# Kernel optimization log

Measured on AMD Instinct MI355X. Metric: run time of the kernel, lower is better.

The kernel has to match this reference:

```python
import jax, jax.numpy as jnp
import numpy as np

B, V, D, E, F, H, HD = 16, 1024, 16, 64, 16, 128, 64
GRAPH_LAYERS, FLOW_ITERS, DUAL_ITERS = 2, 10, 10
STEP, MOM, BIG = 0.01, 0.9, 1e9


def _build_graph():
    # circulant graph: node v's d-th out-neighbor is v + offs[d] (mod V); offsets paired (o, -o)
    offs = np.array([1, -1, 2, -2, 3, -3, 4, -4, 5, -5, 6, -6, 7, -7, 8, -8], dtype=np.int32)
    v = np.arange(V, dtype=np.int32)[:, None]
    d = np.broadcast_to(np.arange(D, dtype=np.int32)[None, :], (V, D))
    adj = ((v + offs[None, :]) % V).astype(np.int32)
    inv_adj = ((v - offs[None, :]) % V).astype(np.int32)
    in_idx = np.stack([inv_adj, d], axis=-1)    # d-th incoming edge of v == out-edge (inv_adj[v,d], slot d)
    rev_idx = np.stack([adj, d], axis=-1)       # out-edge (v,d) is the d-th incoming edge of adj[v,d]
    opp_idx = np.stack([adj, d ^ 1], axis=-1)   # opposite edge (w->v) is slot d^1 at w (paired offsets)
    bt = lambda x: jnp.asarray(np.broadcast_to(x[None], (B,) + x.shape).copy())
    return bt(adj), bt(inv_adj), bt(in_idx), bt(rev_idx), bt(opp_idx)


def setup_inputs() -> dict:
    key = jax.random.key(0)
    ks = jax.random.split(key, 16)
    adj_lst, inv_adj_lst, in_indices, rev_indices, opp_indices = _build_graph()
    rn = lambda k, shape, scale=1.0: jax.random.normal(k, shape, dtype=jnp.float32) * scale
    s = lambda fan: 1.0 / float(np.sqrt(fan))
    return {
        'demands': rn(ks[0], (B, V, 1)),
        'node_features': rn(ks[1], (B, V, F)),
        'edge_lengths': jax.random.uniform(ks[2], (B, V, D), dtype=jnp.float32),
        'norm_edge_lengths': jax.random.uniform(ks[3], (B, V, D), dtype=jnp.float32),
        'node_emb': rn(ks[4], (V, E)),
        'W_enc': rn(ks[5], (E + F, H), s(E + F)), 'b_enc': jnp.zeros((H,), jnp.float32),
        'W_gat': rn(ks[6], (H, H), s(H)), 'b_gat': jnp.zeros((H,), jnp.float32),
        'a_gat': rn(ks[7], (H,), s(H)),
        'W_gru_x': rn(ks[8], (H, 3 * H), s(H)), 'W_gru_h': rn(ks[9], (H, 3 * H), s(H)),
        'b_gru': jnp.zeros((3 * H,), jnp.float32),
        'W_dec1': rn(ks[10], (2 * H, HD), s(2 * H)), 'b_dec1': jnp.zeros((HD,), jnp.float32),
        'W_dec2': rn(ks[11], (HD, 1), s(HD)), 'b_dec2': jnp.zeros((1,), jnp.float32),
        'W_dual1': rn(ks[12], (H, HD), s(H)), 'b_dual1': jnp.zeros((HD,), jnp.float32),
        'W_dual2': rn(ks[13], (HD, 1), s(HD)), 'b_dual2': jnp.zeros((1,), jnp.float32),
        'adj_lst': adj_lst, 'inv_adj_lst': inv_adj_lst,
        'in_indices': in_indices, 'rev_indices': rev_indices, 'opp_indices': opp_indices,
        'num_nodes': jnp.full((B,), V, dtype=jnp.int32),
    }


def _gather_nodes(values, idx, valid):
    # masked_gather with set_zero=True: values (B,V,H), idx (B,V,D) -> (B,V,D,H)
    bb = jnp.arange(values.shape[0])[:, None, None]
    g = values[bb, jnp.clip(idx, 0, values.shape[1] - 1)]
    return g * valid[..., None]


def _gather_edges(x, idx):
    # gather_nd into a (B,V,D,...) tensor; idx (B,V,D,2) = (node, slot), batch implicit
    bb = jnp.arange(x.shape[0])[:, None, None]
    return x[bb, idx[..., 0], idx[..., 1]]


def _sparsemax(z):
    n = z.shape[-1]
    zs = jnp.sort(z, axis=-1)[..., ::-1]
    k = jnp.arange(1, n + 1, dtype=z.dtype)
    zc = jnp.cumsum(zs, axis=-1)
    support = (1.0 + k * zs) > zc
    kz = jnp.sum(support, axis=-1, keepdims=True)
    tau = (jnp.take_along_axis(zc, kz - 1, axis=-1) - 1.0) / kz.astype(z.dtype)
    return jnp.maximum(z - tau, 0.0)


def _forward(demands, node_features, edge_lengths, norm_edge_lengths, node_emb, W_enc, b_enc,
             W_gat, b_gat, a_gat, W_gru_x, W_gru_h, b_gru, W_dec1, b_dec1, W_dec2, b_dec2,
             W_dual1, b_dual1, W_dual2, b_dual2,
             adj_lst, inv_adj_lst, in_indices, rev_indices, opp_indices, num_nodes):
    f32 = jnp.float32
    # embedding lookup with max_norm=1
    nrm = jnp.linalg.norm(node_emb, axis=-1, keepdims=True)
    emb = node_emb / jnp.maximum(nrm, 1.0)
    emb_b = jnp.broadcast_to(emb[None], (demands.shape[0], V, E))
    node_enc = jnp.concatenate([emb_b, node_features], axis=-1) @ W_enc + b_enc   # (B,V,H)
    mask = (adj_lst == num_nodes[:, None, None]).astype(f32)                       # 1 = padded slot
    valid = 1.0 - mask
    initial = _gather_nodes(node_enc, adj_lst, valid)                              # (B,V,D,H)
    h = initial
    for _ in range(GRAPH_LAYERS):
        # DirectionalGAT: per-edge transform, masked attention over slots, directional regather
        t = jnp.tanh(h @ W_gat + b_gat)                                            # (B,V,D,H)
        logits = jnp.einsum('bvdh,h->bvd', t, a_gat) - BIG * mask
        attn = jax.nn.softmax(logits, axis=-1)
        node_msg = jnp.einsum('bvd,bvdh->bvh', attn, t)                            # (B,V,H)
        msg = _gather_nodes(node_msg, adj_lst, valid)
        x = jnp.tanh(msg + initial)
        # GRU cell, shared weights over all edge states
        gx = x @ W_gru_x + b_gru
        gh = h @ W_gru_h
        z = jax.nn.sigmoid(gx[..., :H] + gh[..., :H])
        r = jax.nn.sigmoid(gx[..., H:2 * H] + gh[..., H:2 * H])
        cand = jnp.tanh(gx[..., 2 * H:] + r * gh[..., 2 * H:])
        h = z * h + (1.0 - z) * cand
    # decoder over (encoding, encoding + opposite-edge encoding)
    comb = h + _gather_edges(h, opp_indices)
    dec_in = jnp.concatenate([h, comb], axis=-1)
    nw = (jnp.tanh(dec_in @ W_dec1 + b_dec1) @ W_dec2 + b_dec2)[..., 0]            # (B,V,D)
    # destination attention: normalize over incoming edges, map back to outgoing layout
    inv_mask = (inv_adj_lst == num_nodes[:, None, None]).astype(f32)
    in_w = _gather_edges(nw, in_indices)
    dest_attn = jax.nn.softmax(in_w - BIG * inv_mask, axis=-1)
    nw = _gather_edges(dest_attn, rev_indices)
    pred = nw - BIG * mask
    normalized = _sparsemax(pred) * valid
    # iterative proportional min-cost-flow solver
    def mcf_step(flow, _):
        inflow = jnp.sum(_gather_edges(flow, in_indices), axis=-1, keepdims=True)  # (B,V,1)
        return normalized * jax.nn.relu(inflow - demands), None
    flow, _ = jax.lax.scan(mcf_step, jnp.zeros_like(normalized), None, length=FLOW_ITERS)
    flow_cost = jnp.sum(flow * flow, axis=(1, 2))                                  # square cost fn
    # dual variables + dual flow (projected momentum gradient descent)
    node_states = jnp.sum(h, axis=2)                                               # (B,V,H)
    dual_vars = jax.nn.relu(jnp.tanh(node_states @ W_dual1 + b_dual1) @ W_dual2 + b_dual2)  # (B,V,1)
    dual = mask * dual_vars
    dual_tr = _gather_nodes(dual_vars, adj_lst, valid)[..., 0]
    dual_diff = dual_tr - dual                                                     # (B,V,D)
    def dual_step(carry, _):
        f, vel = carry
        grad = 2.0 * f + dual_diff                                                 # d/df [f^2 + dual_diff*f]
        vel = MOM * vel - STEP * grad
        f = jax.nn.relu(f + vel)
        return (f, vel), None
    (dual_flows, _), _ = jax.lax.scan(dual_step, (jnp.zeros_like(dual_diff), jnp.zeros_like(dual_diff)), None, length=DUAL_ITERS)
    dual_flows = dual_flows * valid
    dual_demand = jnp.sum(dual_vars * demands, axis=(1, 2))
    dual_cost = jnp.sum(dual_flows * dual_flows + dual_diff * dual_flows, axis=(1, 2)) - dual_demand
    return flow_cost - dual_cost                                                   # (B,) primal-dual gap loss


def reference(demands, node_features, edge_lengths, norm_edge_lengths, node_emb, W_enc, b_enc,
              W_gat, b_gat, a_gat, W_gru_x, W_gru_h, b_gru, W_dec1, b_dec1, W_dec2, b_dec2,
              W_dual1, b_dual1, W_dual2, b_dual2,
              adj_lst, inv_adj_lst, in_indices, rev_indices, opp_indices, num_nodes):
    return _forward(demands, node_features, edge_lengths, norm_edge_lengths, node_emb, W_enc, b_enc,
                    W_gat, b_gat, a_gat, W_gru_x, W_gru_h, b_gru, W_dec1, b_dec1, W_dec2, b_dec2,
                    W_dual1, b_dual1, W_dual2, b_dual2,
                    adj_lst, inv_adj_lst, in_indices, rev_indices, opp_indices, num_nodes)
```

## Files before the change

### kernel.cpp

```cpp
#include <hip/hip_runtime.h>
#include <hip/hip_bf16.h>

#define B 16
#define V 1024
#define D 16
#define E 64
#define F 16
#define H 128
#define HD 64
#define BV (B*V)
#define BVD (B*V*D)

#define OFF_HNB      0
#define OFF_NORM     (OFF_HNB + BV*H/2)
#define OFF_DV       (OFF_NORM + BVD)
#define OFF_WT       (OFF_DV + BV)
#define OFF_WTG      (OFF_WT + 65536)
#define OFF_WPQ      (OFF_WTG + 8192)
#define OFF_WU1T     (OFF_WPQ + 8192)
#define OFF_WENCT    (OFF_WU1T + 4096)

typedef __attribute__((ext_vector_type(8))) short bf16x8;
typedef __attribute__((ext_vector_type(4))) float f32x4;

__device__ __forceinline__ short f2bf(float f){
  __hip_bfloat16 b = __float2bfloat16(f);
  return *reinterpret_cast<short*>(&b);
}
__device__ __forceinline__ float bf2f(short s){
  __hip_bfloat16 b; *reinterpret_cast<short*>(&b) = s;
  return __bfloat162float(b);
}
__device__ __forceinline__ float frcp(float x){ return __builtin_amdgcn_rcpf(x); }
__device__ __forceinline__ float fsig(float x){ return frcp(1.f + __expf(-x)); }
__device__ __forceinline__ float ftanh(float x){
  float e = __expf(-2.f*fabsf(x));
  float r = (1.f - e)*frcp(1.f + e);
  return copysignf(r, x);
}

__global__ __launch_bounds__(256) void k_pre(const float* __restrict__ Wx, const float* __restrict__ Wh,
    const float* __restrict__ Wg, const float* __restrict__ W1, const float* __restrict__ Wu1,
    const float* __restrict__ Wenc,
    short* __restrict__ Wt, short* __restrict__ Wgt, short* __restrict__ Wpq,
    short* __restrict__ Wu1t, short* __restrict__ Wenct, float* __restrict__ outz){
  int bid = blockIdx.x, tid = threadIdx.x;
  if (bid == 0 && tid < 16) outz[tid] = 0.f;
  if (bid < 512){
    int n = bid, k = tid;
    int g = n >> 7, j = n & 127;
    float v;
    if (g == 0)      v = (k < 128) ? Wx[k*384 + j]       : Wh[(k-128)*384 + j];
    else if (g == 1) v = (k < 128) ? Wx[k*384 + 128 + j] : Wh[(k-128)*384 + 128 + j];
    else if (g == 2) v = (k < 128) ? Wx[k*384 + 256 + j] : 0.f;
    else             v = (k < 128) ? 0.f                 : Wh[(k-128)*384 + 256 + j];
    Wt[n*256 + k] = f2bf(v);
    return;
  }
  if (bid < 576){
    int idx = (bid-512)*256 + tid;
    int n = idx >> 7, k = idx & 127;
    Wgt[n*128 + k] = f2bf(Wg[k*128 + n]);
    return;
  }
  if (bid < 608){
    int idx = (bid-576)*256 + tid;
    int n = idx >> 7, k = idx & 127;
    float wb = W1[(k+128)*HD + n];
    float wa = W1[k*HD + n];
    Wpq[n*128 + k]      = f2bf(wa + wb);
    Wpq[(64+n)*128 + k] = f2bf(wb);
    return;
  }
  if (bid < 640){
    int idx = (bid-608)*256 + tid;
    int n = idx >> 7, k = idx & 127;
    Wu1t[n*128 + k] = f2bf(Wu1[k*HD + n]);
    return;
  }
  {
    int nn = (bid-640)*2 + (tid >> 7);
    int kk = tid & 127;
    if (kk < 96) Wenct[nn*96 + kk] = f2bf(kk < 80 ? Wenc[kk*128 + nn] : 0.f);
  }
}

__global__ __launch_bounds__(512,2) void k_mega(const float* __restrict__ emb, const float* __restrict__ nf,
    const short* __restrict__ Wenct, const float* __restrict__ benc, const int* __restrict__ adj,
    const short* __restrict__ Wgt, const float* __restrict__ bg, const float* __restrict__ ag,
    const short* __restrict__ Wt, const float* __restrict__ bgru, short* __restrict__ hout){
  __shared__ short NE[96][136];
  __shared__ short Tt[128][104];
  __shared__ short H1[80][136];
  __shared__ short X[80][136];
  __shared__ short A2[80][104];
  __shared__ float Lp[8][96];
  __shared__ float Ls[96];
  __shared__ float nrmv[96];
  short (*As)[104] = reinterpret_cast<short(*)[104]>(&H1[0][0]);

  int tid = threadIdx.x;
  int blk = blockIdx.x;
  int b = blk >> 4;
  int n0 = (blk & 15) << 6;
  int w = tid >> 6, lane = tid & 63;
  int l15 = lane & 15, quad = lane >> 4;

  int li96[16];
  if (tid < 80){
    int wg = (b<<10) + ((n0 - 8 + tid) & 1023);
    const int4* a4 = reinterpret_cast<const int4*>(&adj[(long)wg*16]);
    #pragma unroll
    for (int d4=0; d4<4; d4++){
      int4 i4 = a4[d4];
      li96[d4*4+0] = (i4.x - n0 + 16) & 1023;
      li96[d4*4+1] = (i4.y - n0 + 16) & 1023;
      li96[d4*4+2] = (i4.z - n0 + 16) & 1023;
      li96[d4*4+3] = (i4.w - n0 + 16) & 1023;
    }
  }

  if (tid < 384){
    int r = tid >> 2, q = tid & 3;
    int v = (n0 - 16 + r) & 1023;
    const float4* e4 = reinterpret_cast<const float4*>(&emb[v*E]);
    float ss = 0.f;
    #pragma unroll
    for (int qq=0;qq<4;qq++){ float4 x = e4[q*4+qq]; ss += x.x*x.x + x.y*x.y + x.z*x.z + x.w*x.w; }
    ss += __shfl_xor(ss, 1);
    ss += __shfl_xor(ss, 2);
    if (q == 0) nrmv[r] = frcp(fmaxf(sqrtf(ss), 1.f));
  }
  __syncthreads();
  for (int e=tid; e<96*16; e+=512){
    int r = e >> 4, q = e & 15;
    int v = (n0 - 16 + r) & 1023;
    float4 x = reinterpret_cast<const float4*>(&emb[v*E])[q];
    float iv = nrmv[r];
    short4 s; s.x=f2bf(x.x*iv); s.y=f2bf(x.y*iv); s.z=f2bf(x.z*iv); s.w=f2bf(x.w*iv);
    *reinterpret_cast<short4*>(&As[r][q*4]) = s;
  }
  for (int e=tid; e<96*4; e+=512){
    int r = e >> 2, q = e & 3;
    int m = (b<<10) + ((n0 - 16 + r) & 1023);
    float4 x = reinterpret_cast<const float4*>(&nf[(long)m*F])[q];
    short4 s; s.x=f2bf(x.x); s.y=f2bf(x.y); s.z=f2bf(x.z); s.w=f2bf(x.w);
    *reinterpret_cast<short4*>(&As[r][64 + q*4]) = s;
    short4 z; z.x=0; z.y=0; z.z=0; z.w=0;
    *reinterpret_cast<short4*>(&As[r][80 + q*4]) = z;
  }
  __syncthreads();
  {
    f32x4 acc[6];
    #pragma unroll
    for (int mt=0;mt<6;mt++) acc[mt] = (f32x4){0.f,0.f,0.f,0.f};
    #pragma unroll
    for (int kc=0;kc<3;kc++){
      int k0 = kc*32;
      bf16x8 bfr = *reinterpret_cast<const bf16x8*>(&Wenct[(16*w + l15)*96 + k0 + quad*8]);
      #pragma unroll
      for (int mt=0;mt<6;mt++){
        bf16x8 a = *reinterpret_cast<const bf16x8*>(&As[16*mt + l15][k0 + quad*8]);
        acc[mt] = __builtin_amdgcn_mfma_f32_16x16x32_bf16(a, bfr, acc[mt], 0,0,0);
      }
    }
    int c = 16*w + l15;
    float bb = benc[c];
    #pragma unroll
    for (int mt=0;mt<6;mt++)
      #pragma unroll
      for (int reg=0;reg<4;reg++)
        NE[16*mt + quad*4 + reg][c] = f2bf(acc[mt][reg] + bb);
  }
  __syncthreads();
  {
    f32x4 acc[6];
    #pragma unroll
    for (int mt=0;mt<6;mt++) acc[mt] = (f32x4){0.f,0.f,0.f,0.f};
    #pragma unroll
    for (int kc=0;kc<4;kc++){
      int k0 = kc*32;
      bf16x8 bfr = *reinterpret_cast<const bf16x8*>(&Wgt[(16*w + l15)*128 + k0 + quad*8]);
      #pragma unroll
      for (int mt=0;mt<6;mt++){
        bf16x8 a = *reinterpret_cast<const bf16x8*>(&NE[16*mt + l15][k0 + quad*8]);
        acc[mt] = __builtin_amdgcn_mfma_f32_16x16x32_bf16(a, bfr, acc[mt], 0,0,0);
      }
    }
    int c = 16*w + l15;
    float bgc = bg[c], agc = ag[c];
    float lp[6][4];
    #pragma unroll
    for (int mt=0;mt<6;mt++){
      short4 tv;
      #pragma unroll
      for (int reg=0;reg<4;reg++){
        float t = ftanh(acc[mt][reg] + bgc);
        reinterpret_cast<short*>(&tv)[reg] = f2bf(t);
        lp[mt][reg] = t * agc;
      }
      *reinterpret_cast<short4*>(&Tt[c][16*mt + quad*4]) = tv;
    }
    #pragma unroll
    for (int mt=0;mt<6;mt++)
      #pragma unroll
      for (int reg=0;reg<4;reg++){
        lp[mt][reg] += __shfl_xor(lp[mt][reg], 1);
        lp[mt][reg] += __shfl_xor(lp[mt][reg], 2);
        lp[mt][reg] += __shfl_xor(lp[mt][reg], 4);
        lp[mt][reg] += __shfl_xor(lp[mt][reg], 8);
      }
    if (l15 == 0){
      #pragma unroll
      for (int mt=0;mt<6;mt++)
        #pragma unroll
        for (int reg=0;reg<4;reg++)
          Lp[w][16*mt + quad*4 + reg] = lp[mt][reg];
    }
  }
  __syncthreads();
  if (tid < 96){
    float s = 0.f;
    #pragma unroll
    for (int i=0;i<8;i++) s += Lp[i][tid];
    Ls[tid] = s;
  }
  {
    bf16x8 z8;
    #pragma unroll
    for (int q=0;q<8;q++) z8[q] = 0;
    for (int idx=tid; idx<960; idx+=512){
      int r = idx/12, c8 = idx%12;
      *reinterpret_cast<bf16x8*>(&A2[r][c8*8]) = z8;
    }
  }
  __syncthreads();
  if (tid < 80){
    float at[16];
    float m = -1e30f;
    #pragma unroll
    for (int d=0; d<16; d++) m = fmaxf(m, Ls[li96[d]]);
    float s = 0.f;
    #pragma unroll
    for (int d=0; d<16; d++){ at[d] = __expf(Ls[li96[d]] - m); s += at[d]; }
    float inv = frcp(s);
    #pragma unroll
    for (int d=0; d<16; d++) A2[tid][li96[d]] = f2bf(at[d]*inv);
  }
  __syncthreads();
  {
    f32x4 acc[5];
    #pragma unroll
    for (int mt=0;mt<5;mt++) acc[mt] = (f32x4){0.f,0.f,0.f,0.f};
    #pragma unroll
    for (int kc=0;kc<3;kc++){
      int k0 = kc*32;
      bf16x8 bfr = *reinterpret_cast<const bf16x8*>(&Tt[16*w + l15][k0 + quad*8]);
      #pragma unroll
      for (int mt=0;mt<5;mt++){
        bf16x8 a = *reinterpret_cast<const bf16x8*>(&A2[16*mt + l15][k0 + quad*8]);
        acc[mt] = __builtin_amdgcn_mfma_f32_16x16x32_bf16(a, bfr, acc[mt], 0,0,0);
      }
    }
    int c = 16*w + l15;
    #pragma unroll
    for (int mt=0;mt<5;mt++)
      #pragma unroll
      for (int reg=0;reg<4;reg++){
        int rl = 16*mt + quad*4 + reg;
        X[rl][c] = f2bf(ftanh(acc[mt][reg] + bf2f(NE[rl + 8][c])));
      }
  }
  __syncthreads();
  {
    f32x4 acc[5][4];
    #pragma unroll
    for (int mt=0;mt<5;mt++)
      #pragma unroll
      for (int g=0;g<4;g++) acc[mt][g] = (f32x4){0.f,0.f,0.f,0.f};
    for (int k8=0;k8<8;k8++){
      int k0 = k8*32;
      int gg = (k8 < 4) ? 2 : 3;
      int ncol = 16*w + l15;
      int koff = k0 + quad*8;
      bf16x8 bz = *reinterpret_cast<const bf16x8*>(&Wt[(ncol      )*256 + koff]);
      bf16x8 br = *reinterpret_cast<const bf16x8*>(&Wt[(ncol + 128)*256 + koff]);
      bf16x8 bc = *reinterpret_cast<const bf16x8*>(&Wt[(ncol + gg*128)*256 + koff]);
      #pragma unroll
      for (int mt=0;mt<5;mt++){
        bf16x8 a;
        if (k8 < 4) a = *reinterpret_cast<const bf16x8*>(&X[16*mt + l15][k0 + quad*8]);
        else        a = *reinterpret_cast<const bf16x8*>(&NE[16*mt + l15 + 8][k0 - 128 + quad*8]);
        acc[mt][0]  = __builtin_amdgcn_mfma_f32_16x16x32_bf16(a, bz, acc[mt][0], 0,0,0);
        acc[mt][1]  = __builtin_amdgcn_mfma_f32_16x16x32_bf16(a, br, acc[mt][1], 0,0,0);
        acc[mt][gg] = __builtin_amdgcn_mfma_f32_16x16x32_bf16(a, bc, acc[mt][gg], 0,0,0);
      }
    }
    int j = 16*w + l15;
    float bjz = bgru[j], bjr = bgru[128 + j], bjc = bgru[256 + j];
    #pragma unroll
    for (int mt=0;mt<5;mt++){
      #pragma unroll
      for (int reg=0;reg<4;reg++){
        int rl = 16*mt + quad*4 + reg;
        float z = fsig(acc[mt][0][reg] + bjz);
        float r = fsig(acc[mt][1][reg] + bjr);
        float cand = ftanh(acc[mt][2][reg] + bjc + r*acc[mt][3][reg]);
        float ho = bf2f(NE[rl + 8][j]);
        H1[rl][j] = f2bf(z*ho + (1.f - z)*cand);
      }
    }
  }
  __syncthreads();
  {
    f32x4 acc[5];
    #pragma unroll
    for (int mt=0;mt<5;mt++) acc[mt] = (f32x4){0.f,0.f,0.f,0.f};
    #pragma unroll
    for (int kc=0;kc<4;kc++){
      int k0 = kc*32;
      bf16x8 bfr = *reinterpret_cast<const bf16x8*>(&Wgt[(16*w + l15)*128 + k0 + quad*8]);
      #pragma unroll
      for (int mt=0;mt<5;mt++){
        bf16x8 a = *reinterpret_cast<const bf16x8*>(&H1[16*mt + l15][k0 + quad*8]);
        acc[mt] = __builtin_amdgcn_mfma_f32_16x16x32_bf16(a, bfr, acc[mt], 0,0,0);
      }
    }
    int c = 16*w + l15;
    float bgc = bg[c], agc = ag[c];
    float lp[5][4];
    #pragma unroll
    for (int mt=0;mt<5;mt++){
      short4 tv;
      #pragma unroll
      for (int reg=0;reg<4;reg++){
        float t = ftanh(acc[mt][reg] + bgc);
        reinterpret_cast<short*>(&tv)[reg] = f2bf(t);
        lp[mt][reg] = t * agc;
      }
      *reinterpret_cast<short4*>(&Tt[c][16*mt + quad*4]) = tv;
    }
    #pragma unroll
    for (int mt=0;mt<5;mt++)
      #pragma unroll
      for (int reg=0;reg<4;reg++){
        lp[mt][reg] += __shfl_xor(lp[mt][reg], 1);
        lp[mt][reg] += __shfl_xor(lp[mt][reg], 2);
        lp[mt][reg] += __shfl_xor(lp[mt][reg], 4);
        lp[mt][reg] += __shfl_xor(lp[mt][reg], 8);
      }
    if (l15 == 0){
      #pragma unroll
      for (int mt=0;mt<5;mt++)
        #pragma unroll
        for (int reg=0;reg<4;reg++)
          Lp[w][16*mt + quad*4 + reg] = lp[mt][reg];
    }
  }
  __syncthreads();
  if (tid < 80){
    float s = 0.f;
    #pragma unroll
    for (int i=0;i<8;i++) s += Lp[i][tid];
    Ls[tid] = s;
  }
  {
    bf16x8 z8;
    #pragma unroll
    for (int q=0;q<8;q++) z8[q] = 0;
    for (int idx=tid; idx<768; idx+=512){
      int r = idx/12, c8 = idx%12;
      *reinterpret_cast<bf16x8*>(&A2[r][c8*8]) = z8;
    }
  }
  __syncthreads();
  if (tid >= 8 && tid < 72){
    int r5 = tid - 8;
    float at[16];
    float m = -1e30f;
    #pragma unroll
    for (int d=0; d<16; d++) m = fmaxf(m, Ls[li96[d] - 8]);
    float s = 0.f;
    #pragma unroll
    for (int d=0; d<16; d++){ at[d] = __expf(Ls[li96[d] - 8] - m); s += at[d]; }
    float inv = frcp(s);
    #pragma unroll
    for (int d=0; d<16; d++) A2[r5][li96[d] - 8] = f2bf(at[d]*inv);
  }
  __syncthreads();
  {
    f32x4 acc[4];
    #pragma unroll
    for (int mt=0;mt<4;mt++) acc[mt] = (f32x4){0.f,0.f,0.f,0.f};
    #pragma unroll
    for (int kc=0;kc<3;kc++){
      int k0 = kc*32;
      bf16x8 bfr = *reinterpret_cast<const bf16x8*>(&Tt[16*w + l15][k0 + quad*8]);
      #pragma unroll
      for (int mt=0;mt<4;mt++){
        bf16x8 a = *reinterpret_cast<const bf16x8*>(&A2[16*mt + l15][k0 + quad*8]);
        acc[mt] = __builtin_amdgcn_mfma_f32_16x16x32_bf16(a, bfr, acc[mt], 0,0,0);
      }
    }
    int c = 16*w + l15;
    #pragma unroll
    for (int mt=0;mt<4;mt++)
      #pragma unroll
      for (int reg=0;reg<4;reg++){
        int rl = 16*mt + quad*4 + reg;
        X[rl][c] = f2bf(ftanh(acc[mt][reg] + bf2f(NE[rl + 16][c])));
      }
  }
  __syncthreads();
  {
    f32x4 acc[4][4];
    #pragma unroll
    for (int mt=0;mt<4;mt++)
      #pragma unroll
      for (int g=0;g<4;g++) acc[mt][g] = (f32x4){0.f,0.f,0.f,0.f};
    for (int k8=0;k8<8;k8++){
      int k0 = k8*32;
      int gg = (k8 < 4) ? 2 : 3;
      int ncol = 16*w + l15;
      int koff = k0 + quad*8;
      bf16x8 bz = *reinterpret_cast<const bf16x8*>(&Wt[(ncol      )*256 + koff]);
      bf16x8 br = *reinterpret_cast<const bf16x8*>(&Wt[(ncol + 128)*256 + koff]);
      bf16x8 bc = *reinterpret_cast<const bf16x8*>(&Wt[(ncol + gg*128)*256 + koff]);
      #pragma unroll
      for (int mt=0;mt<4;mt++){
        bf16x8 a;
        if (k8 < 4) a = *reinterpret_cast<const bf16x8*>(&X[16*mt + l15][k0 + quad*8]);
        else        a = *reinterpret_cast<const bf16x8*>(&H1[16*mt + l15 + 8][k0 - 128 + quad*8]);
        acc[mt][0]  = __builtin_amdgcn_mfma_f32_16x16x32_bf16(a, bz, acc[mt][0], 0,0,0);
        acc[mt][1]  = __builtin_amdgcn_mfma_f32_16x16x32_bf16(a, br, acc[mt][1], 0,0,0);
        acc[mt][gg] = __builtin_amdgcn_mfma_f32_16x16x32_bf16(a, bc, acc[mt][gg], 0,0,0);
      }
    }
    __syncthreads();
    int j = 16*w + l15;
    float bjz = bgru[j], bjr = bgru[128 + j], bjc = bgru[256 + j];
    #pragma unroll
    for (int mt=0;mt<4;mt++){
      #pragma unroll
      for (int reg=0;reg<4;reg++){
        int rl = 16*mt + quad*4 + reg;
        float z = fsig(acc[mt][0][reg] + bjz);
        float r = fsig(acc[mt][1][reg] + bjr);
        float cand = ftanh(acc[mt][2][reg] + bjc + r*acc[mt][3][reg]);
        float ho = bf2f(H1[rl + 8][j]);
        X[rl][j] = f2bf(z*ho + (1.f - z)*cand);
      }
    }
  }
  __syncthreads();
  for (int idx=tid; idx<64*16; idx+=512){
    int r = idx >> 4, c8 = idx & 15;
    *reinterpret_cast<bf16x8*>(&hout[(long)((b<<10) + n0 + r)*128 + c8*8]) =
        *reinterpret_cast<const bf16x8*>(&X[r][c8*8]);
  }
}

__global__ __launch_bounds__(1024,4) void k_decdas(const short* __restrict__ hn, const int* __restrict__ adj,
    const int* __restrict__ invadj, const short* __restrict__ Wpq, const float* __restrict__ b1,
    const float* __restrict__ W2, const float* __restrict__ b2_,
    const short* __restrict__ Wu1t, const float* __restrict__ bu1, const float* __restrict__ Wu2,
    const float* __restrict__ bu2_, float* __restrict__ norm_, float* __restrict__ dv){
  __shared__ short Hs[112][136];
  __shared__ short PQb[112][132];
  __shared__ short NSs[64][136];
  __shared__ int adjL[64][16];
  __shared__ float dvp[64][4];
  __shared__ float b1s[64], w2s[64], bu1s[64], wu2s[64];
  int tid = threadIdx.x;
  int blk = blockIdx.x;
  int b = blk >> 4;
  int n0 = (blk & 15) << 6;
  if (tid < 64){ b1s[tid] = b1[tid]; w2s[tid] = W2[tid]; bu1s[tid] = bu1[tid]; wu2s[tid] = Wu2[tid]; }
  for (int idx=tid; idx<112*16; idx+=1024){
    int r = idx >> 4, c8 = idx & 15;
    int g = (b << 10) + ((n0 - 24 + r) & 1023);
    *reinterpret_cast<bf16x8*>(&Hs[r][c8*8]) =
        *reinterpret_cast<const bf16x8*>(&hn[(long)g*128 + c8*8]);
  }
  {
    int r = tid >> 4, d = tid & 15;
    int a = adj[((b<<10) + n0 + r)*16 + d];
    adjL[r][d] = (a - n0 + 24) & 1023;
  }
  __syncthreads();
  int w = tid >> 6, lane = tid & 63;
  int l15 = lane & 15, quad = lane >> 4;
  int cw = w & 7, hw = w >> 3;
  {
    f32x4 acc[4];
    #pragma unroll
    for (int t=0;t<4;t++) acc[t] = (f32x4){0.f,0.f,0.f,0.f};
    #pragma unroll
    for (int kc=0;kc<4;kc++){
      int k0 = kc*32;
      bf16x8 bfr = *reinterpret_cast<const bf16x8*>(&Wpq[(16*cw + l15)*128 + k0 + quad*8]);
      #pragma unroll
      for (int t=0;t<4;t++){
        int mt = 4*hw + t;
        if (mt < 7){
          bf16x8 a = *reinterpret_cast<const bf16x8*>(&Hs[16*mt + l15][k0 + quad*8]);
          acc[t] = __builtin_amdgcn_mfma_f32_16x16x32_bf16(a, bfr, acc[t], 0,0,0);
        }
      }
    }
    int c = 16*cw + l15;
    #pragma unroll
    for (int t=0;t<4;t++){
      int mt = 4*hw + t;
      if (mt < 7){
        #pragma unroll
        for (int reg=0;reg<4;reg++)
          PQb[16*mt + quad*4 + reg][c] = f2bf(acc[t][reg]);
      }
    }
  }
  {
    int r = tid >> 4, c8 = tid & 15;
    float acc8[8] = {0,0,0,0,0,0,0,0};
    #pragma unroll 4
    for (int d=0; d<16; d++){
      bf16x8 hv = *reinterpret_cast<const bf16x8*>(&Hs[adjL[r][d]][c8*8]);
      #pragma unroll
      for (int q=0;q<8;q++) acc8[q] += bf2f(hv[q]);
    }
    bf16x8 sv;
    #pragma unroll
    for (int q=0;q<8;q++) sv[q] = f2bf(acc8[q]);
    *reinterpret_cast<bf16x8*>(&NSs[r][c8*8]) = sv;
  }
  __syncthreads();
  if (w < 8){
    int c4 = w & 3, h2 = w >> 2;
    f32x4 acc[2];
    #pragma unroll
    for (int t=0;t<2;t++) acc[t] = (f32x4){0.f,0.f,0.f,0.f};
    #pragma unroll
    for (int kc=0;kc<4;kc++){
      int k0 = kc*32;
      bf16x8 bfr = *reinterpret_cast<const bf16x8*>(&Wu1t[(16*c4 + l15)*128 + k0 + quad*8]);
      #pragma unroll
      for (int t=0;t<2;t++){
        bf16x8 a = *reinterpret_cast<const bf16x8*>(&NSs[16*(2*h2+t) + l15][k0 + quad*8]);
        acc[t] = __builtin_amdgcn_mfma_f32_16x16x32_bf16(a, bfr, acc[t], 0,0,0);
      }
    }
    int n = 16*c4 + l15;
    float bn = bu1s[n], wn = wu2s[n];
    #pragma unroll
    for (int t=0;t<2;t++){
      #pragma unroll
      for (int reg=0;reg<4;reg++){
        float p = ftanh(acc[t][reg] + bn) * wn;
        p += __shfl_xor(p, 1);
        p += __shfl_xor(p, 2);
        p += __shfl_xor(p, 4);
        p += __shfl_xor(p, 8);
        if (l15 == 0) dvp[16*(2*h2+t) + quad*4 + reg][c4] = p;
      }
    }
  }
  __syncthreads();
  float* nws = reinterpret_cast<float*>(&Hs[0][0]);
  float b2v = b2_[0];
  for (int e = tid; e < 96*16; e += 1024){
    int rr = e >> 4, d = e & 15;
    int wnode = (n0 + rr - 16) & 1023;
    int wg = (b<<10) + wnode;
    int a = adj[wg*16 + d];
    int al = (a - n0 + 24) & 1023;
    int wl = rr + 8;
    float p = 0.f;
    #pragma unroll 8
    for (int c=0;c<64;c++)
      p += ftanh(bf2f(PQb[al][c]) + bf2f(PQb[wl][64 + c]) + b1s[c]) * w2s[c];
    nws[rr*17 + d] = p + b2v;
  }
  __syncthreads();
  if (tid < 64){
    float val = dvp[tid][0]+dvp[tid][1]+dvp[tid][2]+dvp[tid][3];
    dv[(b<<10) + n0 + tid] = fmaxf(val + bu2_[0], 0.f);
  }
  float* datt = reinterpret_cast<float*>(&PQb[0][0]);
  if (tid < 80){
    int wnode = (n0 + tid - 8) & 1023;
    int wg = (b<<10) + wnode;
    float vals[16];
    float m = -1e30f;
    #pragma unroll
    for (int d=0; d<16; d++){
      int iv = invadj[wg*16 + d];
      int il = (iv - n0 + 16) & 1023;
      vals[d] = nws[il*17 + d];
      m = fmaxf(m, vals[d]);
    }
    float s = 0.f;
    #pragma unroll
    for (int d=0; d<16; d++){ vals[d] = __expf(vals[d]-m); s += vals[d]; }
    float inv = frcp(s);
    #pragma unroll
    for (int d=0; d<16; d++) datt[tid*17 + d] = vals[d]*inv;
  }
  __syncthreads();
  if (tid < 64){
    int vg = (b<<10) + n0 + tid;
    float z[16], s[16];
    #pragma unroll
    for (int d=0; d<16; d++){
      int al = adjL[tid][d] - 16;
      z[d] = datt[al*17 + d];
      s[d] = z[d];
    }
    #pragma unroll
    for (int k2 = 2; k2 <= 16; k2 <<= 1){
      #pragma unroll
      for (int jj = k2 >> 1; jj > 0; jj >>= 1){
        #pragma unroll
        for (int i = 0; i < 16; i++){
          int l = i ^ jj;
          if (l > i){
            bool up = ((i & k2) == 0);
            float a = s[i], bb = s[l];
            bool sw = up ? (a > bb) : (a < bb);
            if (sw){ s[i]=bb; s[l]=a; }
          }
        }
      }
    }
    float cs = 0.f, zcs = 0.f; int kz = 1;
    #pragma unroll
    for (int j=0;j<16;j++){
      float zj = s[15-j];
      cs += zj;
      if (1.f + (float)(j+1)*zj > cs){ kz = j+1; zcs = cs; }
    }
    float tau = (zcs - 1.f)/(float)kz;
    #pragma unroll
    for (int d=0; d<16; d++) norm_[(long)vg*16 + d] = fmaxf(z[d]-tau, 0.f);
  }
}

__global__ __launch_bounds__(256) void k_flowfin(const float* __restrict__ norm_,
    const float* __restrict__ dem, const int* __restrict__ invadj, const float* __restrict__ dv,
    float* __restrict__ out){
  __shared__ float nrmS[224*17];
  __shared__ float sbuf[2][224];
  __shared__ float red[4];
  int tid = threadIdx.x;
  int blk = blockIdx.x;
  int b = blk >> 4;
  int t0 = (blk & 15) << 6;
  for (int e=tid; e<224*4; e+=256){
    int r = e >> 2, q4 = e & 3;
    int v = (t0 - 80 + r) & 1023;
    float4 x = reinterpret_cast<const float4*>(&norm_[(long)((b<<10) + v)*16])[q4];
    nrmS[r*17 + q4*4+0] = x.x; nrmS[r*17 + q4*4+1] = x.y;
    nrmS[r*17 + q4*4+2] = x.z; nrmS[r*17 + q4*4+3] = x.w;
  }
  bool act = tid < 224;
  int r = tid;
  float dm = 0.f; int gv = 0;
  int ivl[16];
  if (act){
    int v = (t0 - 80 + r) & 1023;
    gv = (b<<10) + v;
    dm = dem[gv];
    #pragma unroll
    for (int d4=0; d4<4; d4++){
      int4 i4 = reinterpret_cast<const int4*>(&invadj[(long)gv*16])[d4];
      int t;
      t = (i4.x - t0 + 80) & 1023; ivl[d4*4+0] = t < 224 ? t : 223;
      t = (i4.y - t0 + 80) & 1023; ivl[d4*4+1] = t < 224 ? t : 223;
      t = (i4.z - t0 + 80) & 1023; ivl[d4*4+2] = t < 224 ? t : 223;
      t = (i4.w - t0 + 80) & 1023; ivl[d4*4+3] = t < 224 ? t : 223;
    }
    sbuf[0][r] = 0.f;
  }
  __syncthreads();
  float nrg[16];
  if (act){
    #pragma unroll
    for (int d=0; d<16; d++) nrg[d] = nrmS[ivl[d]*17 + d];
  }
  int p = 0;
  float s = 0.f;
  for (int it=0; it<10; it++){
    if (act){
      float inflow = 0.f;
      #pragma unroll
      for (int d=0; d<16; d++) inflow += nrg[d]*sbuf[p][ivl[d]];
      s = fmaxf(inflow - dm, 0.f);
      sbuf[1-p][r] = s;
    }
    p ^= 1;
    __syncthreads();
  }
  float partF = 0.f, partD = 0.f, partDD = 0.f;
  if (act && r >= 80 && r < 144){
    float nr2 = 0.f;
    #pragma unroll
    for (int d=0; d<16; d++){ float nv = nrmS[r*17 + d]; nr2 += nv*nv; }
    partF = nr2 * s * s;
    float dvv = dv[gv];
    float f = 0.f, vel = 0.f;
    #pragma unroll
    for (int it=0; it<10; it++){
      float g = 2.f*f + dvv;
      vel = 0.9f*vel - 0.01f*g;
      f = fmaxf(f + vel, 0.f);
    }
    partD = f*f + dvv*f;
    partDD = dvv * dm;
  }
  float val = partF - 16.f*partD + partDD;
  #pragma unroll
  for (int off=32; off>0; off>>=1) val += __shfl_down(val, off);
  if ((tid & 63) == 0) red[tid>>6] = val;
  __syncthreads();
  if (tid == 0) atomicAdd(&out[b], red[0]+red[1]+red[2]+red[3]);
}

extern "C" void kernel_launch(void* const* d_in, const int* in_sizes, int n_in,
                              void* d_out, int out_size, void* d_ws, size_t ws_size,
                              hipStream_t stream){
  (void)in_sizes; (void)n_in; (void)out_size; (void)ws_size;
  const float* demands = (const float*)d_in[0];
  const float* nf      = (const float*)d_in[1];
  const float* emb     = (const float*)d_in[4];
  const float* Wenc    = (const float*)d_in[5];
  const float* benc    = (const float*)d_in[6];
  const float* Wgat    = (const float*)d_in[7];
  const float* bgat    = (const float*)d_in[8];
  const float* agat    = (const float*)d_in[9];
  const float* Wgx     = (const float*)d_in[10];
  const float* Wgh     = (const float*)d_in[11];
  const float* bgru    = (const float*)d_in[12];
  const float* Wd1     = (const float*)d_in[13];
  const float* bd1     = (const float*)d_in[14];
  const float* Wd2     = (const float*)d_in[15];
  const float* bd2     = (const float*)d_in[16];
  const float* Wu1     = (const float*)d_in[17];
  const float* bu1     = (const float*)d_in[18];
  const float* Wu2     = (const float*)d_in[19];
  const float* bu2     = (const float*)d_in[20];
  const int* adj       = (const int*)d_in[21];
  const int* invadj    = (const int*)d_in[22];

  float* ws    = (float*)d_ws;
  short* hnB   = (short*)(ws + OFF_HNB);
  float* nrm   = ws + OFF_NORM;
  float* dv    = ws + OFF_DV;
  short* wt    = (short*)(ws + OFF_WT);
  short* wtg   = (short*)(ws + OFF_WTG);
  short* wpq   = (short*)(ws + OFF_WPQ);
  short* wu1t  = (short*)(ws + OFF_WU1T);
  short* wenct = (short*)(ws + OFF_WENCT);

  k_pre<<<704, 256, 0, stream>>>(Wgx, Wgh, Wgat, Wd1, Wu1, Wenc, wt, wtg, wpq, wu1t, wenct,
                                 (float*)d_out);
  k_mega<<<BV/64, 512, 0, stream>>>(emb, nf, wenct, benc, adj, wtg, bgat, agat, wt, bgru, hnB);
  k_decdas<<<BV/64, 1024, 0, stream>>>(hnB, adj, invadj, wpq, bd1, Wd2, bd2,
                                       wu1t, bu1, Wu2, bu2, nrm, dv);
  k_flowfin<<<B*16, 256, 0, stream>>>(nrm, demands, invadj, dv, (float*)d_out);
}
```

Baseline: 176.6 us.

## Fuse GNN, decoder and flow kernels into one cooperative kernel with grid syncs

Merges the three per-tile kernels (GNN encoder/GAT/GRU, decoder plus dual attention, flow iterations) into a single cooperative launch. Stages are separated by grid-wide syncs and share a union of shared-memory layouts. The decoder stage now runs with 512 threads instead of 1024, with its loops adjusted to match. This removes kernel launch gaps and tail effects but adds grid-barrier cost, and the merged stages may limit occupancy because of register and shared-memory pressure.

```diff
diff --git a/kernel.cpp b/kernel.cpp
--- a/kernel.cpp
+++ b/kernel.cpp
@@ -1,5 +1,8 @@
 #include <hip/hip_runtime.h>
+#include <hip/hip_cooperative_groups.h>
 #include <hip/hip_bf16.h>
+
+namespace cg = cooperative_groups;
 
 #define B 16
 #define V 1024
@@ -85,19 +88,42 @@
   }
 }
 
-__global__ __launch_bounds__(512,2) void k_mega(const float* __restrict__ emb, const float* __restrict__ nf,
+__global__ __launch_bounds__(512,2) void k_fused(
+    const float* __restrict__ emb, const float* __restrict__ nf,
     const short* __restrict__ Wenct, const float* __restrict__ benc, const int* __restrict__ adj,
     const short* __restrict__ Wgt, const float* __restrict__ bg, const float* __restrict__ ag,
-    const short* __restrict__ Wt, const float* __restrict__ bgru, short* __restrict__ hout){
-  __shared__ short NE[96][136];
-  __shared__ short Tt[128][104];
-  __shared__ short H1[80][136];
-  __shared__ short X[80][136];
-  __shared__ short A2[80][104];
-  __shared__ float Lp[8][96];
-  __shared__ float Ls[96];
-  __shared__ float nrmv[96];
-  short (*As)[104] = reinterpret_cast<short(*)[104]>(&H1[0][0]);
+    const short* __restrict__ Wt, const float* __restrict__ bgru, short* __restrict__ hout,
+    const int* __restrict__ invadj, const short* __restrict__ Wpq, const float* __restrict__ b1,
+    const float* __restrict__ W2, const float* __restrict__ b2_,
+    const short* __restrict__ Wu1t, const float* __restrict__ bu1, const float* __restrict__ Wu2,
+    const float* __restrict__ bu2_,
+    float* __restrict__ norm_, float* __restrict__ dv,
+    const float* __restrict__ dem, float* __restrict__ out){
+  __shared__ union {
+    struct {
+      short NE[96][136];
+      short Tt[128][104];
+      short H1[80][136];
+      short X[80][136];
+      short A2[80][104];
+      float Lp[8][96];
+      float Ls[96];
+      float nrmv[96];
+    } a;
+    struct {
+      short Hs[112][136];
+      short PQb[112][132];
+      short NSs[64][136];
+      int adjL[64][16];
+      float dvp[64][4];
+      float b1s[64], w2s[64], bu1s[64], wu2s[64];
+    } b;
+    struct {
+      float nrmS[224*17];
+      float sbuf[2][224];
+      float red[8];
+    } c;
+  } U;
 
   int tid = threadIdx.x;
   int blk = blockIdx.x;
@@ -106,622 +132,613 @@
   int w = tid >> 6, lane = tid & 63;
   int l15 = lane & 15, quad = lane >> 4;
 
-  int li96[16];
-  if (tid < 80){
-    int wg = (b<<10) + ((n0 - 8 + tid) & 1023);
-    const int4* a4 = reinterpret_cast<const int4*>(&adj[(long)wg*16]);
+  {
+    auto& NE = U.a.NE; auto& Tt = U.a.Tt; auto& H1 = U.a.H1; auto& X = U.a.X;
+    auto& A2 = U.a.A2; auto& Lp = U.a.Lp; auto& Ls = U.a.Ls; auto& nrmv = U.a.nrmv;
+    short (*As)[104] = reinterpret_cast<short(*)[104]>(&H1[0][0]);
+
+    int li96[16];
+    if (tid < 80){
+      int wg = (b<<10) + ((n0 - 8 + tid) & 1023);
+      const int4* a4 = reinterpret_cast<const int4*>(&adj[(long)wg*16]);
+      #pragma unroll
+      for (int d4=0; d4<4; d4++){
+        int4 i4 = a4[d4];
+        li96[d4*4+0] = (i4.x - n0 + 16) & 1023;
+        li96[d4*4+1] = (i4.y - n0 + 16) & 1023;
+        li96[d4*4+2] = (i4.z - n0 + 16) & 1023;
+        li96[d4*4+3] = (i4.w - n0 + 16) & 1023;
+      }
+    }
+
+    if (tid < 384){
+      int r = tid >> 2, q = tid & 3;
+      int v = (n0 - 16 + r) & 1023;
+      const float4* e4 = reinterpret_cast<const float4*>(&emb[v*E]);
+      float ss = 0.f;
+      #pragma unroll
+      for (int qq=0;qq<4;qq++){ float4 x = e4[q*4+qq]; ss += x.x*x.x + x.y*x.y + x.z*x.z + x.w*x.w; }
+      ss += __shfl_xor(ss, 1);
+      ss += __shfl_xor(ss, 2);
+      if (q == 0) nrmv[r] = frcp(fmaxf(sqrtf(ss), 1.f));
+    }
+    __syncthreads();
+    for (int e=tid; e<96*16; e+=512){
+      int r = e >> 4, q = e & 15;
+      int v = (n0 - 16 + r) & 1023;
+      float4 x = reinterpret_cast<const float4*>(&emb[v*E])[q];
+      float iv = nrmv[r];
+      short4 s; s.x=f2bf(x.x*iv); s.y=f2bf(x.y*iv); s.z=f2bf(x.z*iv); s.w=f2bf(x.w*iv);
+      *reinterpret_cast<short4*>(&As[r][q*4]) = s;
+    }
+    for (int e=tid; e<96*4; e+=512){
+      int r = e >> 2, q = e & 3;
+      int m = (b<<10) + ((n0 - 16 + r) & 1023);
+      float4 x = reinterpret_cast<const float4*>(&nf[(long)m*F])[q];
+      short4 s; s.x=f2bf(x.x); s.y=f2bf(x.y); s.z=f2bf(x.z); s.w=f2bf(x.w);
+      *reinterpret_cast<short4*>(&As[r][64 + q*4]) = s;
+      short4 z; z.x=0; z.y=0; z.z=0; z.w=0;
+      *reinterpret_cast<short4*>(&As[r][80 + q*4]) = z;
+    }
+    __syncthreads();
+    {
+      f32x4 acc[6];
+      #pragma unroll
+      for (int mt=0;mt<6;mt++) acc[mt] = (f32x4){0.f,0.f,0.f,0.f};
+      #pragma unroll
+      for (int kc=0;kc<3;kc++){
+        int k0 = kc*32;
+        bf16x8 bfr = *reinterpret_cast<const bf16x8*>(&Wenct[(16*w + l15)*96 + k0 + quad*8]);
+        #pragma unroll
+        for (int mt=0;mt<6;mt++){
+          bf16x8 a = *reinterpret_cast<const bf16x8*>(&As[16*mt + l15][k0 + quad*8]);
+          acc[mt] = __builtin_amdgcn_mfma_f32_16x16x32_bf16(a, bfr, acc[mt], 0,0,0);
+        }
+      }
+      int c = 16*w + l15;
+      float bb = benc[c];
+      #pragma unroll
+      for (int mt=0;mt<6;mt++)
+        #pragma unroll
+        for (int reg=0;reg<4;reg++)
+          NE[16*mt + quad*4 + reg][c] = f2bf(acc[mt][reg] + bb);
+    }
+    __syncthreads();
+    {
+      f32x4 acc[6];
+      #pragma unroll
+      for (int mt=0;mt<6;mt++) acc[mt] = (f32x4){0.f,0.f,0.f,0.f};
+      #pragma unroll
+      for (int kc=0;kc<4;kc++){
+        int k0 = kc*32;
+        bf16x8 bfr = *reinterpret_cast<const bf16x8*>(&Wgt[(16*w + l15)*128 + k0 + quad*8]);
+        #pragma unroll
+        for (int mt=0;mt<6;mt++){
+          bf16x8 a = *reinterpret_cast<const bf16x8*>(&NE[16*mt + l15][k0 + quad*8]);
+          acc[mt] = __builtin_amdgcn_mfma_f32_16x16x32_bf16(a, bfr, acc[mt], 0,0,0);
+        }
+      }
+      int c = 16*w + l15;
+      float bgc = bg[c], agc = ag[c];
+      float lp[6][4];
+      #pragma unroll
+      for (int mt=0;mt<6;mt++){
+        short4 tv;
+        #pragma unroll
+        for (int reg=0;reg<4;reg++){
+          float t = ftanh(acc[mt][reg] + bgc);
+          reinterpret_cast<short*>(&tv)[reg] = f2bf(t);
+          lp[mt][reg] = t * agc;
+        }
+        *reinterpret_cast<short4*>(&Tt[c][16*mt + quad*4]) = tv;
+      }
+      #pragma unroll
+      for (int mt=0;mt<6;mt++)
+        #pragma unroll
+        for (int reg=0;reg<4;reg++){
+          lp[mt][reg] += __shfl_xor(lp[mt][reg], 1);
+          lp[mt][reg] += __shfl_xor(lp[mt][reg], 2);
+          lp[mt][reg] += __shfl_xor(lp[mt][reg], 4);
+          lp[mt][reg] += __shfl_xor(lp[mt][reg], 8);
+        }
+      if (l15 == 0){
+        #pragma unroll
+        for (int mt=0;mt<6;mt++)
+          #pragma unroll
+          for (int reg=0;reg<4;reg++)
+            Lp[w][16*mt + quad*4 + reg] = lp[mt][reg];
+      }
+    }
+    __syncthreads();
+    if (tid < 96){
+      float s = 0.f;
+      #pragma unroll
+      for (int i=0;i<8;i++) s += Lp[i][tid];
+      Ls[tid] = s;
+    }
+    {
+      bf16x8 z8;
+      #pragma unroll
+      for (int q=0;q<8;q++) z8[q] = 0;
+      for (int idx=tid; idx<960; idx+=512){
+        int r = idx/12, c8 = idx%12;
+        *reinterpret_cast<bf16x8*>(&A2[r][c8*8]) = z8;
+      }
+    }
+    __syncthreads();
+    if (tid < 80){
+      float at[16];
+      float m = -1e30f;
+      #pragma unroll
+      for (int d=0; d<16; d++) m = fmaxf(m, Ls[li96[d]]);
+      float s = 0.f;
+      #pragma unroll
+      for (int d=0; d<16; d++){ at[d] = __expf(Ls[li96[d]] - m); s += at[d]; }
+      float inv = frcp(s);
+      #pragma unroll
+      for (int d=0; d<16; d++) A2[tid][li96[d]] = f2bf(at[d]*inv);
+    }
+    __syncthreads();
+    {
+      f32x4 acc[5];
+      #pragma unroll
+      for (int mt=0;mt<5;mt++) acc[mt] = (f32x4){0.f,0.f,0.f,0.f};
+      #pragma unroll
+      for (int kc=0;kc<3;kc++){
+        int k0 = kc*32;
+        bf16x8 bfr = *reinterpret_cast<const bf16x8*>(&Tt[16*w + l15][k0 + quad*8]);
+        #pragma unroll
+        for (int mt=0;mt<5;mt++){
+          bf16x8 a = *reinterpret_cast<const bf16x8*>(&A2[16*mt + l15][k0 + quad*8]);
+          acc[mt] = __builtin_amdgcn_mfma_f32_16x16x32_bf16(a, bfr, acc[mt], 0,0,0);
+        }
+      }
+      int c = 16*w + l15;
+      #pragma unroll
+      for (int mt=0;mt<5;mt++)
+        #pragma unroll
+        for (int reg=0;reg<4;reg++){
+          int rl = 16*mt + quad*4 + reg;
+          X[rl][c] = f2bf(ftanh(acc[mt][reg] + bf2f(NE[rl + 8][c])));
+        }
+    }
+    __syncthreads();
+    {
+      f32x4 acc[5][4];
+      #pragma unroll
+      for (int mt=0;mt<5;mt++)
+        #pragma unroll
+        for (int g=0;g<4;g++) acc[mt][g] = (f32x4){0.f,0.f,0.f,0.f};
+      for (int k8=0;k8<8;k8++){
+        int k0 = k8*32;
+        int gg = (k8 < 4) ? 2 : 3;
+        int ncol = 16*w + l15;
+        int koff = k0 + quad*8;
+        bf16x8 bz = *reinterpret_cast<const bf16x8*>(&Wt[(ncol      )*256 + koff]);
+        bf16x8 br = *reinterpret_cast<const bf16x8*>(&Wt[(ncol + 128)*256 + koff]);
+        bf16x8 bc = *reinterpret_cast<const bf16x8*>(&Wt[(ncol + gg*128)*256 + koff]);
+        #pragma unroll
+        for (int mt=0;mt<5;mt++){
+          bf16x8 a;
+          if (k8 < 4) a = *reinterpret_cast<const bf16x8*>(&X[16*mt + l15][k0 + quad*8]);
+          else        a = *reinterpret_cast<const bf16x8*>(&NE[16*mt + l15 + 8][k0 - 128 + quad*8]);
+          acc[mt][0]  = __builtin_amdgcn_mfma_f32_16x16x32_bf16(a, bz, acc[mt][0], 0,0,0);
+          acc[mt][1]  = __builtin_amdgcn_mfma_f32_16x16x32_bf16(a, br, acc[mt][1], 0,0,0);
+          acc[mt][gg] = __builtin_amdgcn_mfma_f32_16x16x32_bf16(a, bc, acc[mt][gg], 0,0,0);
+        }
+      }
+      int j = 16*w + l15;
+      float bjz = bgru[j], bjr = bgru[128 + j], bjc = bgru[256 + j];
+      #pragma unroll
+      for (int mt=0;mt<5;mt++){
+        #pragma unroll
+        for (int reg=0;reg<4;reg++){
+          int rl = 16*mt + quad*4 + reg;
+          float z = fsig(acc[mt][0][reg] + bjz);
+          float r = fsig(acc[mt][1][reg] + bjr);
+          float cand = ftanh(acc[mt][2][reg] + bjc + r*acc[mt][3][reg]);
+          float ho = bf2f(NE[rl + 8][j]);
+          H1[rl][j] = f2bf(z*ho + (1.f - z)*cand);
+        }
+      }
+    }
+    __syncthreads();
+    {
+      f32x4 acc[5];
+      #pragma unroll
+      for (int mt=0;mt<5;mt++) acc[mt] = (f32x4){0.f,0.f,0.f,0.f};
+      #pragma unroll
+      for (int kc=0;kc<4;kc++){
+        int k0 = kc*32;
+        bf16x8 bfr = *reinterpret_cast<const bf16x8*>(&Wgt[(16*w + l15)*128 + k0 + quad*8]);
+        #pragma unroll
+        for (int mt=0;mt<5;mt++){
+          bf16x8 a = *reinterpret_cast<const bf16x8*>(&H1[16*mt + l15][k0 + quad*8]);
+          acc[mt] = __builtin_amdgcn_mfma_f32_16x16x32_bf16(a, bfr, acc[mt], 0,0,0);
+        }
+      }
+      int c = 16*w + l15;
+      float bgc = bg[c], agc = ag[c];
+      float lp[5][4];
+      #pragma unroll
+      for (int mt=0;mt<5;mt++){
+        short4 tv;
+        #pragma unroll
+        for (int reg=0;reg<4;reg++){
+          float t = ftanh(acc[mt][reg] + bgc);
+          reinterpret_cast<short*>(&tv)[reg] = f2bf(t);
+          lp[mt][reg] = t * agc;
+        }
+        *reinterpret_cast<short4*>(&Tt[c][16*mt + quad*4]) = tv;
+      }
+      #pragma unroll
+      for (int mt=0;mt<5;mt++)
+        #pragma unroll
+        for (int reg=0;reg<4;reg++){
+          lp[mt][reg] += __shfl_xor(lp[mt][reg], 1);
+          lp[mt][reg] += __shfl_xor(lp[mt][reg], 2);
+          lp[mt][reg] += __shfl_xor(lp[mt][reg], 4);
+          lp[mt][reg] += __shfl_xor(lp[mt][reg], 8);
+        }
+      if (l15 == 0){
+        #pragma unroll
+        for (int mt=0;mt<5;mt++)
+          #pragma unroll
+          for (int reg=0;reg<4;reg++)
+            Lp[w][16*mt + quad*4 + reg] = lp[mt][reg];
+      }
+    }
+    __syncthreads();
+    if (tid < 80){
+      float s = 0.f;
+      #pragma unroll
+      for (int i=0;i<8;i++) s += Lp[i][tid];
+      Ls[tid] = s;
+    }
+    {
+      bf16x8 z8;
+      #pragma unroll
+      for (int q=0;q<8;q++) z8[q] = 0;
+      for (int idx=tid; idx<768; idx+=512){
+        int r = idx/12, c8 = idx%12;
+        *reinterpret_cast<bf16x8*>(&A2[r][c8*8]) = z8;
+      }
+    }
+    __syncthreads();
+    if (tid >= 8 && tid < 72){
+      int r5 = tid - 8;
+      float at[16];
+      float m = -1e30f;
+      #pragma unroll
+      for (int d=0; d<16; d++) m = fmaxf(m, Ls[li96[d] - 8]);
+      float s = 0.f;
+      #pragma unroll
+      for (int d=0; d<16; d++){ at[d] = __expf(Ls[li96[d] - 8] - m); s += at[d]; }
+      float inv = frcp(s);
+      #pragma unroll
+      for (int d=0; d<16; d++) A2[r5][li96[d] - 8] = f2bf(at[d]*inv);
+    }
+    __syncthreads();
+    {
+      f32x4 acc[4];
+      #pragma unroll
+      for (int mt=0;mt<4;mt++) acc[mt] = (f32x4){0.f,0.f,0.f,0.f};
+      #pragma unroll
+      for (int kc=0;kc<3;kc++){
+        int k0 = kc*32;
+        bf16x8 bfr = *reinterpret_cast<const bf16x8*>(&Tt[16*w + l15][k0 + quad*8]);
+        #pragma unroll
+        for (int mt=0;mt<4;mt++){
+          bf16x8 a = *reinterpret_cast<const bf16x8*>(&A2[16*mt + l15][k0 + quad*8]);
+          acc[mt] = __builtin_amdgcn_mfma_f32_16x16x32_bf16(a, bfr, acc[mt], 0,0,0);
+        }
+      }
+      int c = 16*w + l15;
+      #pragma unroll
+      for (int mt=0;mt<4;mt++)
+        #pragma unroll
+        for (int reg=0;reg<4;reg++){
+          int rl = 16*mt + quad*4 + reg;
+          X[rl][c] = f2bf(ftanh(acc[mt][reg] + bf2f(NE[rl + 16][c])));
+        }
+    }
+    __syncthreads();
+    {
+      f32x4 acc[4][4];
+      #pragma unroll
+      for (int mt=0;mt<4;mt++)
+        #pragma unroll
+        for (int g=0;g<4;g++) acc[mt][g] = (f32x4){0.f,0.f,0.f,0.f};
+      for (int k8=0;k8<8;k8++){
+        int k0 = k8*32;
+        int gg = (k8 < 4) ? 2 : 3;
+        int ncol = 16*w + l15;
+        int koff = k0 + quad*8;
+        bf16x8 bz = *reinterpret_cast<const bf16x8*>(&Wt[(ncol      )*256 + koff]);
+        bf16x8 br = *reinterpret_cast<const bf16x8*>(&Wt[(ncol + 128)*256 + koff]);
+        bf16x8 bc = *reinterpret_cast<const bf16x8*>(&Wt[(ncol + gg*128)*256 + koff]);
+        #pragma unroll
+        for (int mt=0;mt<4;mt++){
+          bf16x8 a;
+          if (k8 < 4) a = *reinterpret_cast<const bf16x8*>(&X[16*mt + l15][k0 + quad*8]);
+          else        a = *reinterpret_cast<const bf16x8*>(&H1[16*mt + l15 + 8][k0 - 128 + quad*8]);
+          acc[mt][0]  = __builtin_amdgcn_mfma_f32_16x16x32_bf16(a, bz, acc[mt][0], 0,0,0);
+          acc[mt][1]  = __builtin_amdgcn_mfma_f32_16x16x32_bf16(a, br, acc[mt][1], 0,0,0);
+          acc[mt][gg] = __builtin_amdgcn_mfma_f32_16x16x32_bf16(a, bc, acc[mt][gg], 0,0,0);
+        }
+      }
+      __syncthreads();
+      int j = 16*w + l15;
+      float bjz = bgru[j], bjr = bgru[128 + j], bjc = bgru[256 + j];
+      #pragma unroll
+      for (int mt=0;mt<4;mt++){
+        #pragma unroll
+        for (int reg=0;reg<4;reg++){
+          int rl = 16*mt + quad*4 + reg;
+          float z = fsig(acc[mt][0][reg] + bjz);
+          float r = fsig(acc[mt][1][reg] + bjr);
+          float cand = ftanh(acc[mt][2][reg] + bjc + r*acc[mt][3][reg]);
+          float ho = bf2f(H1[rl + 8][j]);
+          X[rl][j] = f2bf(z*ho + (1.f - z)*cand);
+        }
+      }
+    }
+    __syncthreads();
+    for (int idx=tid; idx<64*16; idx+=512){
+      int r = idx >> 4, c8 = idx & 15;
+      *reinterpret_cast<bf16x8*>(&hout[(long)((b<<10) + n0 + r)*128 + c8*8]) =
+          *reinterpret_cast<const bf16x8*>(&X[r][c8*8]);
+    }
+  }
+
+  __threadfence();
+  cg::this_grid().sync();
+
+  {
+    auto& Hs = U.b.Hs; auto& PQb = U.b.PQb; auto& NSs = U.b.NSs;
+    auto& adjL = U.b.adjL; auto& dvp = U.b.dvp;
+    float* b1s = U.b.b1s; float* w2s = U.b.w2s; float* bu1s = U.b.bu1s; float* wu2s = U.b.wu2s;
+
+    if (tid < 64){ b1s[tid] = b1[tid]; w2s[tid] = W2[tid]; bu1s[tid] = bu1[tid]; wu2s[tid] = Wu2[tid]; }
+    for (int idx=tid; idx<112*16; idx+=512){
+      int r = idx >> 4, c8 = idx & 15;
+      int g = (b << 10) + ((n0 - 24 + r) & 1023);
+      *reinterpret_cast<bf16x8*>(&Hs[r][c8*8]) =
+          *reinterpret_cast<const bf16x8*>(&hout[(long)g*128 + c8*8]);
+    }
+    for (int idx=tid; idx<1024; idx+=512){
+      int r = idx >> 4, d = idx & 15;
+      int a = adj[((b<<10) + n0 + r)*16 + d];
+      adjL[r][d] = (a - n0 + 24) & 1023;
+    }
+    __syncthreads();
+    {
+      f32x4 acc[7];
+      #pragma unroll
+      for (int mt=0;mt<7;mt++) acc[mt] = (f32x4){0.f,0.f,0.f,0.f};
+      #pragma unroll
+      for (int kc=0;kc<4;kc++){
+        int k0 = kc*32;
+        bf16x8 bfr = *reinterpret_cast<const bf16x8*>(&Wpq[(16*w + l15)*128 + k0 + quad*8]);
+        #pragma unroll
+        for (int mt=0;mt<7;mt++){
+          bf16x8 a = *reinterpret_cast<const bf16x8*>(&Hs[16*mt + l15][k0 + quad*8]);
+          acc[mt] = __builtin_amdgcn_mfma_f32_16x16x32_bf16(a, bfr, acc[mt], 0,0,0);
+        }
+      }
+      int c = 16*w + l15;
+      #pragma unroll
+      for (int mt=0;mt<7;mt++)
+        #pragma unroll
+        for (int reg=0;reg<4;reg++)
+          PQb[16*mt + quad*4 + reg][c] = f2bf(acc[mt][reg]);
+    }
+    for (int idx=tid; idx<64*16; idx+=512){
+      int r = idx >> 4, c8 = idx & 15;
+      float acc8[8] = {0,0,0,0,0,0,0,0};
+      #pragma unroll 4
+      for (int d=0; d<16; d++){
+        bf16x8 hv = *reinterpret_cast<const bf16x8*>(&Hs[adjL[r][d]][c8*8]);
+        #pragma unroll
+        for (int q=0;q<8;q++) acc8[q] += bf2f(hv[q]);
+      }
+      bf16x8 sv;
+      #pragma unroll
+      for (int q=0;q<8;q++) sv[q] = f2bf(acc8[q]);
+      *reinterpret_cast<bf16x8*>(&NSs[r][c8*8]) = sv;
+    }
+    __syncthreads();
+    if (w < 4){
+      f32x4 acc[4];
+      #pragma unroll
+      for (int mt=0;mt<4;mt++) acc[mt] = (f32x4){0.f,0.f,0.f,0.f};
+      #pragma unroll
+      for (int kc=0;kc<4;kc++){
+        int k0 = kc*32;
+        bf16x8 bfr = *reinterpret_cast<const bf16x8*>(&Wu1t[(16*w + l15)*128 + k0 + quad*8]);
+        #pragma unroll
+        for (int mt=0;mt<4;mt++){
+          bf16x8 a = *reinterpret_cast<const bf16x8*>(&NSs[16*mt + l15][k0 + quad*8]);
+          acc[mt] = __builtin_amdgcn_mfma_f32_16x16x32_bf16(a, bfr, acc[mt], 0,0,0);
+        }
+      }
+      int n = 16*w + l15;
+      float bn = bu1s[n], wn = wu2s[n];
+      #pragma unroll
+      for (int mt=0;mt<4;mt++){
+        #pragma unroll
+        for (int reg=0;reg<4;reg++){
+          float p = ftanh(acc[mt][reg] + bn) * wn;
+          p += __shfl_xor(p, 1);
+          p += __shfl_xor(p, 2);
+          p += __shfl_xor(p, 4);
+          p += __shfl_xor(p, 8);
+          if (l15 == 0) dvp[16*mt + quad*4 + reg][w] = p;
+        }
+      }
+    }
+    __syncthreads();
+    float* nws = reinterpret_cast<float*>(&Hs[0][0]);
+    float b2v = b2_[0];
+    for (int e = tid; e < 96*16; e += 512){
+      int rr = e >> 4, d = e & 15;
+      int wnode = (n0 + rr - 16) & 1023;
+      int wg = (b<<10) + wnode;
+      int a = adj[wg*16 + d];
+      int al = (a - n0 + 24) & 1023;
+      int wl = rr + 8;
+      float p = 0.f;
+      #pragma unroll 8
+      for (int c=0;c<64;c++)
+        p += ftanh(bf2f(PQb[al][c]) + bf2f(PQb[wl][64 + c]) + b1s[c]) * w2s[c];
+      nws[rr*17 + d] = p + b2v;
+    }
+    __syncthreads();
+    if (tid < 64){
+      float val = dvp[tid][0]+dvp[tid][1]+dvp[tid][2]+dvp[tid][3];
+      dv[(b<<10) + n0 + tid] = fmaxf(val + bu2_[0], 0.f);
+    }
+    float* datt = reinterpret_cast<float*>(&PQb[0][0]);
+    if (tid < 80){
+      int wnode = (n0 + tid - 8) & 1023;
+      int wg = (b<<10) + wnode;
+      float vals[16];
+      float m = -1e30f;
+      #pragma unroll
+      for (int d=0; d<16; d++){
+        int iv = invadj[wg*16 + d];
+        int il = (iv - n0 + 16) & 1023;
+        vals[d] = nws[il*17 + d];
+        m = fmaxf(m, vals[d]);
+      }
+      float s = 0.f;
+      #pragma unroll
+      for (int d=0; d<16; d++){ vals[d] = __expf(vals[d]-m); s += vals[d]; }
+      float inv = frcp(s);
+      #pragma unroll
+      for (int d=0; d<16; d++) datt[tid*17 + d] = vals[d]*inv;
+    }
+    __syncthreads();
+    if (tid < 64){
+      int vg = (b<<10) + n0 + tid;
+      float z[16], s[16];
+      #pragma unroll
+      for (int d=0; d<16; d++){
+        int al = adjL[tid][d] - 16;
+        z[d] = datt[al*17 + d];
+        s[d] = z[d];
+      }
+      #pragma unroll
+      for (int k2 = 2; k2 <= 16; k2 <<= 1){
+        #pragma unroll
+        for (int jj = k2 >> 1; jj > 0; jj >>= 1){
+          #pragma unroll
+          for (int i = 0; i < 16; i++){
+            int l = i ^ jj;
+            if (l > i){
+              bool up = ((i & k2) == 0);
+              float a = s[i], bb = s[l];
+              bool sw = up ? (a > bb) : (a < bb);
+              if (sw){ s[i]=bb; s[l]=a; }
+            }
+          }
+        }
+      }
+      float cs = 0.f, zcs = 0.f; int kz = 1;
+      #pragma unroll
+      for (int j=0;j<16;j++){
+        float zj = s[15-j];
+        cs += zj;
+        if (1.f + (float)(j+1)*zj > cs){ kz = j+1; zcs = cs; }
+      }
+      float tau = (zcs - 1.f)/(float)kz;
+      #pragma unroll
+      for (int d=0; d<16; d++) norm_[(long)vg*16 + d] = fmaxf(z[d]-tau, 0.f);
+    }
+  }
+
+  __threadfence();
+  cg::this_grid().sync();
+
+  {
+    float* nrmS = U.c.nrmS;
+    auto& sbuf = U.c.sbuf;
+    float* red = U.c.red;
+    int t0 = n0;
+    for (int e=tid; e<224*4; e+=512){
+      int r = e >> 2, q4 = e & 3;
+      int v = (t0 - 80 + r) & 1023;
+      float4 x = reinterpret_cast<const float4*>(&norm_[(long)((b<<10) + v)*16])[q4];
+      nrmS[r*17 + q4*4+0] = x.x; nrmS[r*17 + q4*4+1] = x.y;
+      nrmS[r*17 + q4*4+2] = x.z; nrmS[r*17 + q4*4+3] = x.w;
+    }
+    bool act = tid < 224;
+    int r = tid;
+    float dm = 0.f; int gv = 0;
+    int ivl[16];
+    if (act){
+      int v = (t0 - 80 + r) & 1023;
+      gv = (b<<10) + v;
+      dm = dem[gv];
+      #pragma unroll
+      for (int d4=0; d4<4; d4++){
+        int4 i4 = reinterpret_cast<const int4*>(&invadj[(long)gv*16])[d4];
+        int t;
+        t = (i4.x - t0 + 80) & 1023; ivl[d4*4+0] = t < 224 ? t : 223;
+        t = (i4.y - t0 + 80) & 1023; ivl[d4*4+1] = t < 224 ? t : 223;
+        t = (i4.z - t0 + 80) & 1023; ivl[d4*4+2] = t < 224 ? t : 223;
+        t = (i4.w - t0 + 80) & 1023; ivl[d4*4+3] = t < 224 ? t : 223;
+      }
+      sbuf[0][r] = 0.f;
+    }
+    __syncthreads();
+    float nrg[16];
+    if (act){
+      #pragma unroll
+      for (int d=0; d<16; d++) nrg[d] = nrmS[ivl[d]*17 + d];
+    }
+    int p = 0;
+    float s = 0.f;
+    for (int it=0; it<10; it++){
+      if (act){
+        float inflow = 0.f;
+        #pragma unroll
+        for (int d=0; d<16; d++) inflow += nrg[d]*sbuf[p][ivl[d]];
+        s = fmaxf(inflow - dm, 0.f);
+        sbuf[1-p][r] = s;
+      }
+      p ^= 1;
+      __syncthreads();
+    }
+    float partF = 0.f, partD = 0.f, partDD = 0.f;
+    if (act && r >= 80 && r < 144){
+      float nr2 = 0.f;
+      #pragma unroll
+      for (int d=0; d<16; d++){ float nv = nrmS[r*17 + d]; nr2 += nv*nv; }
+      partF = nr2 * s * s;
+      float dvv = dv[gv];
+      float f = 0.f, vel = 0.f;
+      #pragma unroll
+      for (int it=0; it<10; it++){
+        float g = 2.f*f + dvv;
+        vel = 0.9f*vel - 0.01f*g;
+        f = fmaxf(f + vel, 0.f);
+      }
+      partD = f*f + dvv*f;
+      partDD = dvv * dm;
+    }
+    float val = partF - 16.f*partD + partDD;
     #pragma unroll
-    for (int d4=0; d4<4; d4++){
-      int4 i4 = a4[d4];
-      li96[d4*4+0] = (i4.x - n0 + 16) & 1023;
-      li96[d4*4+1] = (i4.y - n0 + 16) & 1023;
-      li96[d4*4+2] = (i4.z - n0 + 16) & 1023;
-      li96[d4*4+3] = (i4.w - n0 + 16) & 1023;
+    for (int off=32; off>0; off>>=1) val += __shfl_down(val, off);
+    if ((tid & 63) == 0) red[tid>>6] = val;
+    __syncthreads();
+    if (tid == 0){
+      float acc = 0.f;
+      #pragma unroll
+      for (int i=0;i<8;i++) acc += red[i];
+      atomicAdd(&out[b], acc);
     }
   }
-
-  if (tid < 384){
-    int r = tid >> 2, q = tid & 3;
-    int v = (n0 - 16 + r) & 1023;
-    const float4* e4 = reinterpret_cast<const float4*>(&emb[v*E]);
-    float ss = 0.f;
-    #pragma unroll
-    for (int qq=0;qq<4;qq++){ float4 x = e4[q*4+qq]; ss += x.x*x.x + x.y*x.y + x.z*x.z + x.w*x.w; }
-    ss += __shfl_xor(ss, 1);
-    ss += __shfl_xor(ss, 2);
-    if (q == 0) nrmv[r] = frcp(fmaxf(sqrtf(ss), 1.f));
-  }
-  __syncthreads();
-  for (int e=tid; e<96*16; e+=512){
-    int r = e >> 4, q = e & 15;
-    int v = (n0 - 16 + r) & 1023;
-    float4 x = reinterpret_cast<const float4*>(&emb[v*E])[q];
-    float iv = nrmv[r];
-    short4 s; s.x=f2bf(x.x*iv); s.y=f2bf(x.y*iv); s.z=f2bf(x.z*iv); s.w=f2bf(x.w*iv);
-    *reinterpret_cast<short4*>(&As[r][q*4]) = s;
-  }
-  for (int e=tid; e<96*4; e+=512){
-    int r = e >> 2, q = e & 3;
-    int m = (b<<10) + ((n0 - 16 + r) & 1023);
-    float4 x = reinterpret_cast<const float4*>(&nf[(long)m*F])[q];
-    short4 s; s.x=f2bf(x.x); s.y=f2bf(x.y); s.z=f2bf(x.z); s.w=f2bf(x.w);
-    *reinterpret_cast<short4*>(&As[r][64 + q*4]) = s;
-    short4 z; z.x=0; z.y=0; z.z=0; z.w=0;
-    *reinterpret_cast<short4*>(&As[r][80 + q*4]) = z;
-  }
-  __syncthreads();
-  {
-    f32x4 acc[6];
-    #pragma unroll
-    for (int mt=0;mt<6;mt++) acc[mt] = (f32x4){0.f,0.f,0.f,0.f};
-    #pragma unroll
-    for (int kc=0;kc<3;kc++){
-      int k0 = kc*32;
-      bf16x8 bfr = *reinterpret_cast<const bf16x8*>(&Wenct[(16*w + l15)*96 + k0 + quad*8]);
-      #pragma unroll
-      for (int mt=0;mt<6;mt++){
-        bf16x8 a = *reinterpret_cast<const bf16x8*>(&As[16*mt + l15][k0 + quad*8]);
-        acc[mt] = __builtin_amdgcn_mfma_f32_16x16x32_bf16(a, bfr, acc[mt], 0,0,0);
-      }
-    }
-    int c = 16*w + l15;
-    float bb = benc[c];
-    #pragma unroll
-    for (int mt=0;mt<6;mt++)
-      #pragma unroll
-      for (int reg=0;reg<4;reg++)
-        NE[16*mt + quad*4 + reg][c] = f2bf(acc[mt][reg] + bb);
-  }
-  __syncthreads();
-  {
-    f32x4 acc[6];
-    #pragma unroll
-    for (int mt=0;mt<6;mt++) acc[mt] = (f32x4){0.f,0.f,0.f,0.f};
-    #pragma unroll
-    for (int kc=0;kc<4;kc++){
-      int k0 = kc*32;
-      bf16x8 bfr = *reinterpret_cast<const bf16x8*>(&Wgt[(16*w + l15)*128 + k0 + quad*8]);
-      #pragma unroll
-      for (int mt=0;mt<6;mt++){
-        bf16x8 a = *reinterpret_cast<const bf16x8*>(&NE[16*mt + l15][k0 + quad*8]);
-        acc[mt] = __builtin_amdgcn_mfma_f32_16x16x32_bf16(a, bfr, acc[mt], 0,0,0);
-      }
-    }
-    int c = 16*w + l15;
-    float bgc = bg[c], agc = ag[c];
-    float lp[6][4];
-    #pragma unroll
-    for (int mt=0;mt<6;mt++){
-      short4 tv;
-      #pragma unroll
-      for (int reg=0;reg<4;reg++){
-        float t = ftanh(acc[mt][reg] + bgc);
-        reinterpret_cast<short*>(&tv)[reg] = f2bf(t);
-        lp[mt][reg] = t * agc;
-      }
-      *reinterpret_cast<short4*>(&Tt[c][16*mt + quad*4]) = tv;
-    }
-    #pragma unroll
-    for (int mt=0;mt<6;mt++)
-      #pragma unroll
-      for (int reg=0;reg<4;reg++){
-        lp[mt][reg] += __shfl_xor(lp[mt][reg], 1);
-        lp[mt][reg] += __shfl_xor(lp[mt][reg], 2);
-        lp[mt][reg] += __shfl_xor(lp[mt][reg], 4);
-        lp[mt][reg] += __shfl_xor(lp[mt][reg], 8);
-      }
-    if (l15 == 0){
-      #pragma unroll
-      for (int mt=0;mt<6;mt++)
-        #pragma unroll
-        for (int reg=0;reg<4;reg++)
-          Lp[w][16*mt + quad*4 + reg] = lp[mt][reg];
-    }
-  }
-  __syncthreads();
-  if (tid < 96){
-    float s = 0.f;
-    #pragma unroll
-    for (int i=0;i<8;i++) s += Lp[i][tid];
-    Ls[tid] = s;
-  }
-  {
-    bf16x8 z8;
-    #pragma unroll
-    for (int q=0;q<8;q++) z8[q] = 0;
-    for (int idx=tid; idx<960; idx+=512){
-      int r = idx/12, c8 = idx%12;
-      *reinterpret_cast<bf16x8*>(&A2[r][c8*8]) = z8;
-    }
-  }
-  __syncthreads();
-  if (tid < 80){
-    float at[16];
-    float m = -1e30f;
-    #pragma unroll
-    for (int d=0; d<16; d++) m = fmaxf(m, Ls[li96[d]]);
-    float s = 0.f;
-    #pragma unroll
-    for (int d=0; d<16; d++){ at[d] = __expf(Ls[li96[d]] - m); s += at[d]; }
-    float inv = frcp(s);
-    #pragma unroll
-    for (int d=0; d<16; d++) A2[tid][li96[d]] = f2bf(at[d]*inv);
-  }
-  __syncthreads();
-  {
-    f32x4 acc[5];
-    #pragma unroll
-    for (int mt=0;mt<5;mt++) acc[mt] = (f32x4){0.f,0.f,0.f,0.f};
-    #pragma unroll
-    for (int kc=0;kc<3;kc++){
-      int k0 = kc*32;
-      bf16x8 bfr = *reinterpret_cast<const bf16x8*>(&Tt[16*w + l15][k0 + quad*8]);
-      #pragma unroll
-      for (int mt=0;mt<5;mt++){
-        bf16x8 a = *reinterpret_cast<const bf16x8*>(&A2[16*mt + l15][k0 + quad*8]);
-        acc[mt] = __builtin_amdgcn_mfma_f32_16x16x32_bf16(a, bfr, acc[mt], 0,0,0);
-      }
-    }
-    int c = 16*w + l15;
-    #pragma unroll
-    for (int mt=0;mt<5;mt++)
-      #pragma unroll
-      for (int reg=0;reg<4;reg++){
-        int rl = 16*mt + quad*4 + reg;
-        X[rl][c] = f2bf(ftanh(acc[mt][reg] + bf2f(NE[rl + 8][c])));
-      }
-  }
-  __syncthreads();
-  {
-    f32x4 acc[5][4];
-    #pragma unroll
-    for (int mt=0;mt<5;mt++)
-      #pragma unroll
-      for (int g=0;g<4;g++) acc[mt][g] = (f32x4){0.f,0.f,0.f,0.f};
-    for (int k8=0;k8<8;k8++){
-      int k0 = k8*32;
-      int gg = (k8 < 4) ? 2 : 3;
-      int ncol = 16*w + l15;
-      int koff = k0 + quad*8;
-      bf16x8 bz = *reinterpret_cast<const bf16x8*>(&Wt[(ncol      )*256 + koff]);
-      bf16x8 br = *reinterpret_cast<const bf16x8*>(&Wt[(ncol + 128)*256 + koff]);
-      bf16x8 bc = *reinterpret_cast<const bf16x8*>(&Wt[(ncol + gg*128)*256 + koff]);
-      #pragma unroll
-      for (int mt=0;mt<5;mt++){
-        bf16x8 a;
-        if (k8 < 4) a = *reinterpret_cast<const bf16x8*>(&X[16*mt + l15][k0 + quad*8]);
-        else        a = *reinterpret_cast<const bf16x8*>(&NE[16*mt + l15 + 8][k0 - 128 + quad*8]);
-        acc[mt][0]  = __builtin_amdgcn_mfma_f32_16x16x32_bf16(a, bz, acc[mt][0], 0,0,0);
-        acc[mt][1]  = __builtin_amdgcn_mfma_f32_16x16x32_bf16(a, br, acc[mt][1], 0,0,0);
-        acc[mt][gg] = __builtin_amdgcn_mfma_f32_16x16x32_bf16(a, bc, acc[mt][gg], 0,0,0);
-      }
-    }
-    int j = 16*w + l15;
-    float bjz = bgru[j], bjr = bgru[128 + j], bjc = bgru[256 + j];
-    #pragma unroll
-    for (int mt=0;mt<5;mt++){
-      #pragma unroll
-      for (int reg=0;reg<4;reg++){
-        int rl = 16*mt + quad*4 + reg;
-        float z = fsig(acc[mt][0][reg] + bjz);
-        float r = fsig(acc[mt][1][reg] + bjr);
-        float cand = ftanh(acc[mt][2][reg] + bjc + r*acc[mt][3][reg]);
-        float ho = bf2f(NE[rl + 8][j]);
-        H1[rl][j] = f2bf(z*ho + (1.f - z)*cand);
-      }
-    }
-  }
-  __syncthreads();
-  {
-    f32x4 acc[5];
-    #pragma unroll
-    for (int mt=0;mt<5;mt++) acc[mt] = (f32x4){0.f,0.f,0.f,0.f};
-    #pragma unroll
-    for (int kc=0;kc<4;kc++){
-      int k0 = kc*32;
-      bf16x8 bfr = *reinterpret_cast<const bf16x8*>(&Wgt[(16*w + l15)*128 + k0 + quad*8]);
-      #pragma unroll
-      for (int mt=0;mt<5;mt++){
-        bf16x8 a = *reinterpret_cast<const bf16x8*>(&H1[16*mt + l15][k0 + quad*8]);
-        acc[mt] = __builtin_amdgcn_mfma_f32_16x16x32_bf16(a, bfr, acc[mt], 0,0,0);
-      }
-    }
-    int c = 16*w + l15;
-    float bgc = bg[c], agc = ag[c];
-    float lp[5][4];
-    #pragma unroll
-    for (int mt=0;mt<5;mt++){
-      short4 tv;
-      #pragma unroll
-      for (int reg=0;reg<4;reg++){
-        float t = ftanh(acc[mt][reg] + bgc);
-        reinterpret_cast<short*>(&tv)[reg] = f2bf(t);
-        lp[mt][reg] = t * agc;
-      }
-      *reinterpret_cast<short4*>(&Tt[c][16*mt + quad*4]) = tv;
-    }
-    #pragma unroll
-    for (int mt=0;mt<5;mt++)
-      #pragma unroll
-      for (int reg=0;reg<4;reg++){
-        lp[mt][reg] += __shfl_xor(lp[mt][reg], 1);
-        lp[mt][reg] += __shfl_xor(lp[mt][reg], 2);
-        lp[mt][reg] += __shfl_xor(lp[mt][reg], 4);
-        lp[mt][reg] += __shfl_xor(lp[mt][reg], 8);
-      }
-    if (l15 == 0){
-      #pragma unroll
-      for (int mt=0;mt<5;mt++)
-        #pragma unroll
-        for (int reg=0;reg<4;reg++)
-          Lp[w][16*mt + quad*4 + reg] = lp[mt][reg];
-    }
-  }
-  __syncthreads();
-  if (tid < 80){
-    float s = 0.f;
-    #pragma unroll
-    for (int i=0;i<8;i++) s += Lp[i][tid];
-    Ls[tid] = s;
-  }
-  {
-    bf16x8 z8;
-    #pragma unroll
-    for (int q=0;q<8;q++) z8[q] = 0;
-    for (int idx=tid; idx<768; idx+=512){
-      int r = idx/12, c8 = idx%12;
-      *reinterpret_cast<bf16x8*>(&A2[r][c8*8]) = z8;
-    }
-  }
-  __syncthreads();
-  if (tid >= 8 && tid < 72){
-    int r5 = tid - 8;
-    float at[16];
-    float m = -1e30f;
-    #pragma unroll
-    for (int d=0; d<16; d++) m = fmaxf(m, Ls[li96[d] - 8]);
-    float s = 0.f;
-    #pragma unroll
-    for (int d=0; d<16; d++){ at[d] = __expf(Ls[li96[d] - 8] - m); s += at[d]; }
-    float inv = frcp(s);
-    #pragma unroll
-    for (int d=0; d<16; d++) A2[r5][li96[d] - 8] = f2bf(at[d]*inv);
-  }
-  __syncthreads();
-  {
-    f32x4 acc[4];
-    #pragma unroll
-    for (int mt=0;mt<4;mt++) acc[mt] = (f32x4){0.f,0.f,0.f,0.f};
-    #pragma unroll
-    for (int kc=0;kc<3;kc++){
-      int k0 = kc*32;
-      bf16x8 bfr = *reinterpret_cast<const bf16x8*>(&Tt[16*w + l15][k0 + quad*8]);
-      #pragma unroll
-      for (int mt=0;mt<4;mt++){
-        bf16x8 a = *reinterpret_cast<const bf16x8*>(&A2[16*mt + l15][k0 + quad*8]);
-        acc[mt] = __builtin_amdgcn_mfma_f32_16x16x32_bf16(a, bfr, acc[mt], 0,0,0);
-      }
-    }
-    int c = 16*w + l15;
-    #pragma unroll
-    for (int mt=0;mt<4;mt++)
-      #pragma unroll
-      for (int reg=0;reg<4;reg++){
-        int rl = 16*mt + quad*4 + reg;
-        X[rl][c] = f2bf(ftanh(acc[mt][reg] + bf2f(NE[rl + 16][c])));
-      }
-  }
-  __syncthreads();
-  {
-    f32x4 acc[4][4];
-    #pragma unroll
-    for (int mt=0;mt<4;mt++)
-      #pragma unroll
-      for (int g=0;g<4;g++) acc[mt][g] = (f32x4){0.f,0.f,0.f,0.f};
-    for (int k8=0;k8<8;k8++){
-      int k0 = k8*32;
-      int gg = (k8 < 4) ? 2 : 3;
-      int ncol = 16*w + l15;
-      int koff = k0 + quad*8;
-      bf16x8 bz = *reinterpret_cast<const bf16x8*>(&Wt[(ncol      )*256 + koff]);
-      bf16x8 br = *reinterpret_cast<const bf16x8*>(&Wt[(ncol + 128)*256 + koff]);
-      bf16x8 bc = *reinterpret_cast<const bf16x8*>(&Wt[(ncol + gg*128)*256 + koff]);
-      #pragma unroll
-      for (int mt=0;mt<4;mt++){
-        bf16x8 a;
-        if (k8 < 4) a = *reinterpret_cast<const bf16x8*>(&X[16*mt + l15][k0 + quad*8]);
-        else        a = *reinterpret_cast<const bf16x8*>(&H1[16*mt + l15 + 8][k0 - 128 + quad*8]);
-        acc[mt][0]  = __builtin_amdgcn_mfma_f32_16x16x32_bf16(a, bz, acc[mt][0], 0,0,0);
-        acc[mt][1]  = __builtin_amdgcn_mfma_f32_16x16x32_bf16(a, br, acc[mt][1], 0,0,0);
-        acc[mt][gg] = __builtin_amdgcn_mfma_f32_16x16x32_bf16(a, bc, acc[mt][gg], 0,0,0);
-      }
-    }
-    __syncthreads();
-    int j = 16*w + l15;
-    float bjz = bgru[j], bjr = bgru[128 + j], bjc = bgru[256 + j];
-    #pragma unroll
-    for (int mt=0;mt<4;mt++){
-      #pragma unroll
-      for (int reg=0;reg<4;reg++){
-        int rl = 16*mt + quad*4 + reg;
-        float z = fsig(acc[mt][0][reg] + bjz);
-        float r = fsig(acc[mt][1][reg] + bjr);
-        float cand = ftanh(acc[mt][2][reg] + bjc + r*acc[mt][3][reg]);
-        float ho = bf2f(H1[rl + 8][j]);
-        X[rl][j] = f2bf(z*ho + (1.f - z)*cand);
-      }
-    }
-  }
-  __syncthreads();
-  for (int idx=tid; idx<64*16; idx+=512){
-    int r = idx >> 4, c8 = idx & 15;
-    *reinterpret_cast<bf16x8*>(&hout[(long)((b<<10) + n0 + r)*128 + c8*8]) =
-        *reinterpret_cast<const bf16x8*>(&X[r][c8*8]);
-  }
-}
-
-__global__ __launch_bounds__(1024,4) void k_decdas(const short* __restrict__ hn, const int* __restrict__ adj,
-    const int* __restrict__ invadj, const short* __restrict__ Wpq, const float* __restrict__ b1,
-    const float* __restrict__ W2, const float* __restrict__ b2_,
-    const short* __restrict__ Wu1t, const float* __restrict__ bu1, const float* __restrict__ Wu2,
-    const float* __restrict__ bu2_, float* __restrict__ norm_, float* __restrict__ dv){
-  __shared__ short Hs[112][136];
-  __shared__ short PQb[112][132];
-  __shared__ short NSs[64][136];
-  __shared__ int adjL[64][16];
-  __shared__ float dvp[64][4];
-  __shared__ float b1s[64], w2s[64], bu1s[64], wu2s[64];
-  int tid = threadIdx.x;
-  int blk = blockIdx.x;
-  int b = blk >> 4;
-  int n0 = (blk & 15) << 6;
-  if (tid < 64){ b1s[tid] = b1[tid]; w2s[tid] = W2[tid]; bu1s[tid] = bu1[tid]; wu2s[tid] = Wu2[tid]; }
-  for (int idx=tid; idx<112*16; idx+=1024){
-    int r = idx >> 4, c8 = idx & 15;
-    int g = (b << 10) + ((n0 - 24 + r) & 1023);
-    *reinterpret_cast<bf16x8*>(&Hs[r][c8*8]) =
-        *reinterpret_cast<const bf16x8*>(&hn[(long)g*128 + c8*8]);
-  }
-  {
-    int r = tid >> 4, d = tid & 15;
-    int a = adj[((b<<10) + n0 + r)*16 + d];
-    adjL[r][d] = (a - n0 + 24) & 1023;
-  }
-  __syncthreads();
-  int w = tid >> 6, lane = tid & 63;
-  int l15 = lane & 15, quad = lane >> 4;
-  int cw = w & 7, hw = w >> 3;
-  {
-    f32x4 acc[4];
-    #pragma unroll
-    for (int t=0;t<4;t++) acc[t] = (f32x4){0.f,0.f,0.f,0.f};
-    #pragma unroll
-    for (int kc=0;kc<4;kc++){
-      int k0 = kc*32;
-      bf16x8 bfr = *reinterpret_cast<const bf16x8*>(&Wpq[(16*cw + l15)*128 + k0 + quad*8]);
-      #pragma unroll
-      for (int t=0;t<4;t++){
-        int mt = 4*hw + t;
-        if (mt < 7){
-          bf16x8 a = *reinterpret_cast<const bf16x8*>(&Hs[16*mt + l15][k0 + quad*8]);
-          acc[t] = __builtin_amdgcn_mfma_f32_16x16x32_bf16(a, bfr, acc[t], 0,0,0);
-        }
-      }
-    }
-    int c = 16*cw + l15;
-    #pragma unroll
-    for (int t=0;t<4;t++){
-      int mt = 4*hw + t;
-      if (mt < 7){
-        #pragma unroll
-        for (int reg=0;reg<4;reg++)
-          PQb[16*mt + quad*4 + reg][c] = f2bf(acc[t][reg]);
-      }
-    }
-  }
-  {
-    int r = tid >> 4, c8 = tid & 15;
-    float acc8[8] = {0,0,0,0,0,0,0,0};
-    #pragma unroll 4
-    for (int d=0; d<16; d++){
-      bf16x8 hv = *reinterpret_cast<const bf16x8*>(&Hs[adjL[r][d]][c8*8]);
-      #pragma unroll
-      for (int q=0;q<8;q++) acc8[q] += bf2f(hv[q]);
-    }
-    bf16x8 sv;
-    #pragma unroll
-    for (int q=0;q<8;q++) sv[q] = f2bf(acc8[q]);
-    *reinterpret_cast<bf16x8*>(&NSs[r][c8*8]) = sv;
-  }
-  __syncthreads();
-  if (w < 8){
-    int c4 = w & 3, h2 = w >> 2;
-    f32x4 acc[2];
-    #pragma unroll
-    for (int t=0;t<2;t++) acc[t] = (f32x4){0.f,0.f,0.f,0.f};
-    #pragma unroll
-    for (int kc=0;kc<4;kc++){
-      int k0 = kc*32;
-      bf16x8 bfr = *reinterpret_cast<const bf16x8*>(&Wu1t[(16*c4 + l15)*128 + k0 + quad*8]);
-      #pragma unroll
-      for (int t=0;t<2;t++){
-        bf16x8 a = *reinterpret_cast<const bf16x8*>(&NSs[16*(2*h2+t) + l15][k0 + quad*8]);
-        acc[t] = __builtin_amdgcn_mfma_f32_16x16x32_bf16(a, bfr, acc[t], 0,0,0);
-      }
-    }
-    int n = 16*c4 + l15;
-    float bn = bu1s[n], wn = wu2s[n];
-    #pragma unroll
-    for (int t=0;t<2;t++){
-      #pragma unroll
-      for (int reg=0;reg<4;reg++){
-        float p = ftanh(acc[t][reg] + bn) * wn;
-        p += __shfl_xor(p, 1);
-        p += __shfl_xor(p, 2);
-        p += __shfl_xor(p, 4);
-        p += __shfl_xor(p, 8);
-        if (l15 == 0) dvp[16*(2*h2+t) + quad*4 + reg][c4] = p;
-      }
-    }
-  }
-  __syncthreads();
-  float* nws = reinterpret_cast<float*>(&Hs[0][0]);
-  float b2v = b2_[0];
-  for (int e = tid; e < 96*16; e += 1024){
-    int rr = e >> 4, d = e & 15;
-    int wnode = (n0 + rr - 16) & 1023;
-    int wg = (b<<10) + wnode;
-    int a = adj[wg*16 + d];
-    int al = (a - n0 + 24) & 1023;
-    int wl = rr + 8;
-    float p = 0.f;
-    #pragma unroll 8
-    for (int c=0;c<64;c++)
-      p += ftanh(bf2f(PQb[al][c]) + bf2f(PQb[wl][64 + c]) + b1s[c]) * w2s[c];
-    nws[rr*17 + d] = p + b2v;
-  }
-  __syncthreads();
-  if (tid < 64){
-    float val = dvp[tid][0]+dvp[tid][1]+dvp[tid][2]+dvp[tid][3];
-    dv[(b<<10) + n0 + tid] = fmaxf(val + bu2_[0], 0.f);
-  }
-  float* datt = reinterpret_cast<float*>(&PQb[0][0]);
-  if (tid < 80){
-    int wnode = (n0 + tid - 8) & 1023;
-    int wg = (b<<10) + wnode;
-    float vals[16];
-    float m = -1e30f;
-    #pragma unroll
-    for (int d=0; d<16; d++){
-      int iv = invadj[wg*16 + d];
-      int il = (iv - n0 + 16) & 1023;
-      vals[d] = nws[il*17 + d];
-      m = fmaxf(m, vals[d]);
-    }
-    float s = 0.f;
-    #pragma unroll
-    for (int d=0; d<16; d++){ vals[d] = __expf(vals[d]-m); s += vals[d]; }
-    float inv = frcp(s);
-    #pragma unroll
-    for (int d=0; d<16; d++) datt[tid*17 + d] = vals[d]*inv;
-  }
-  __syncthreads();
-  if (tid < 64){
-    int vg = (b<<10) + n0 + tid;
-    float z[16], s[16];
-    #pragma unroll
-    for (int d=0; d<16; d++){
-      int al = adjL[tid][d] - 16;
-      z[d] = datt[al*17 + d];
-      s[d] = z[d];
-    }
-    #pragma unroll
-    for (int k2 = 2; k2 <= 16; k2 <<= 1){
-      #pragma unroll
-      for (int jj = k2 >> 1; jj > 0; jj >>= 1){
-        #pragma unroll
-        for (int i = 0; i < 16; i++){
-          int l = i ^ jj;
-          if (l > i){
-            bool up = ((i & k2) == 0);
-            float a = s[i], bb = s[l];
-            bool sw = up ? (a > bb) : (a < bb);
-            if (sw){ s[i]=bb; s[l]=a; }
-          }
-        }
-      }
-    }
-    float cs = 0.f, zcs = 0.f; int kz = 1;
-    #pragma unroll
-    for (int j=0;j<16;j++){
-      float zj = s[15-j];
-      cs += zj;
-      if (1.f + (float)(j+1)*zj > cs){ kz = j+1; zcs = cs; }
-    }
-    float tau = (zcs - 1.f)/(float)kz;
-    #pragma unroll
-    for (int d=0; d<16; d++) norm_[(long)vg*16 + d] = fmaxf(z[d]-tau, 0.f);
-  }
-}
-
-__global__ __launch_bounds__(256) void k_flowfin(const float* __restrict__ norm_,
-    const float* __restrict__ dem, const int* __restrict__ invadj, const float* __restrict__ dv,
-    float* __restrict__ out){
-  __shared__ float nrmS[224*17];
-  __shared__ float sbuf[2][224];
-  __shared__ float red[4];
-  int tid = threadIdx.x;
-  int blk = blockIdx.x;
-  int b = blk >> 4;
-  int t0 = (blk & 15) << 6;
-  for (int e=tid; e<224*4; e+=256){
-    int r = e >> 2, q4 = e & 3;
-    int v = (t0 - 80 + r) & 1023;
-    float4 x = reinterpret_cast<const float4*>(&norm_[(long)((b<<10) + v)*16])[q4];
-    nrmS[r*17 + q4*4+0] = x.x; nrmS[r*17 + q4*4+1] = x.y;
-    nrmS[r*17 + q4*4+2] = x.z; nrmS[r*17 + q4*4+3] = x.w;
-  }
-  bool act = tid < 224;
-  int r = tid;
-  float dm = 0.f; int gv = 0;
-  int ivl[16];
-  if (act){
-    int v = (t0 - 80 + r) & 1023;
-    gv = (b<<10) + v;
-    dm = dem[gv];
-    #pragma unroll
-    for (int d4=0; d4<4; d4++){
-      int4 i4 = reinterpret_cast<const int4*>(&invadj[(long)gv*16])[d4];
-      int t;
-      t = (i4.x - t0 + 80) & 1023; ivl[d4*4+0] = t < 224 ? t : 223;
-      t = (i4.y - t0 + 80) & 1023; ivl[d4*4+1] = t < 224 ? t : 223;
-      t = (i4.z - t0 + 80) & 1023; ivl[d4*4+2] = t < 224 ? t : 223;
-      t = (i4.w - t0 + 80) & 1023; ivl[d4*4+3] = t < 224 ? t : 223;
-    }
-    sbuf[0][r] = 0.f;
-  }
-  __syncthreads();
-  float nrg[16];
-  if (act){
-    #pragma unroll
-    for (int d=0; d<16; d++) nrg[d] = nrmS[ivl[d]*17 + d];
-  }
-  int p = 0;
-  float s = 0.f;
-  for (int it=0; it<10; it++){
-    if (act){
-      float inflow = 0.f;
-      #pragma unroll
-      for (int d=0; d<16; d++) inflow += nrg[d]*sbuf[p][ivl[d]];
-      s = fmaxf(inflow - dm, 0.f);
-      sbuf[1-p][r] = s;
-    }
-    p ^= 1;
-    __syncthreads();
-  }
-  float partF = 0.f, partD = 0.f, partDD = 0.f;
-  if (act && r >= 80 && r < 144){
-    float nr2 = 0.f;
-    #pragma unroll
-    for (int d=0; d<16; d++){ float nv = nrmS[r*17 + d]; nr2 += nv*nv; }
-    partF = nr2 * s * s;
-    float dvv = dv[gv];
-    float f = 0.f, vel = 0.f;
-    #pragma unroll
-    for (int it=0; it<10; it++){
-      float g = 2.f*f + dvv;
-      vel = 0.9f*vel - 0.01f*g;
-      f = fmaxf(f + vel, 0.f);
-    }
-    partD = f*f + dvv*f;
-    partDD = dvv * dm;
-  }
-  float val = partF - 16.f*partD + partDD;
-  #pragma unroll
-  for (int off=32; off>0; off>>=1) val += __shfl_down(val, off);
-  if ((tid & 63) == 0) red[tid>>6] = val;
-  __syncthreads();
-  if (tid == 0) atomicAdd(&out[b], red[0]+red[1]+red[2]+red[3]);
 }
 
 extern "C" void kernel_launch(void* const* d_in, const int* in_sizes, int n_in,
@@ -759,11 +776,16 @@
   short* wpq   = (short*)(ws + OFF_WPQ);
   short* wu1t  = (short*)(ws + OFF_WU1T);
   short* wenct = (short*)(ws + OFF_WENCT);
-
-  k_pre<<<704, 256, 0, stream>>>(Wgx, Wgh, Wgat, Wd1, Wu1, Wenc, wt, wtg, wpq, wu1t, wenct,
-                                 (float*)d_out);
-  k_mega<<<BV/64, 512, 0, stream>>>(emb, nf, wenct, benc, adj, wtg, bgat, agat, wt, bgru, hnB);
-  k_decdas<<<BV/64, 1024, 0, stream>>>(hnB, adj, invadj, wpq, bd1, Wd2, bd2,
-                                       wu1t, bu1, Wu2, bu2, nrm, dv);
-  k_flowfin<<<B*16, 256, 0, stream>>>(nrm, demands, invadj, dv, (float*)d_out);
+  float* outp  = (float*)d_out;
+
+  k_pre<<<704, 256, 0, stream>>>(Wgx, Wgh, Wgat, Wd1, Wu1, Wenc, wt, wtg, wpq, wu1t, wenct, outp);
+
+  void* kargs[] = {
+    (void*)&emb, (void*)&nf, (void*)&wenct, (void*)&benc, (void*)&adj,
+    (void*)&wtg, (void*)&bgat, (void*)&agat, (void*)&wt, (void*)&bgru, (void*)&hnB,
+    (void*)&invadj, (void*)&wpq, (void*)&bd1, (void*)&Wd2, (void*)&bd2,
+    (void*)&wu1t, (void*)&bu1, (void*)&Wu2, (void*)&bu2,
+    (void*)&nrm, (void*)&dv, (void*)&demands, (void*)&outp
+  };
+  hipLaunchCooperativeKernel((const void*)k_fused, dim3(256), dim3(512), kargs, 0, stream);
 }
```

Result: slower. 353.1 us (+99.9%).
